# Kernel optimization log

Measured on AMD Instinct MI355X. Metric: run time of the kernel, lower is better.

The kernel has to match this reference:

```python
import jax, jax.numpy as jnp
import numpy as np

DIM, HEADS, DH, M, PINV_ITERS, RES_K = 512, 8, 64, 256, 6, 33

def layernorm(x, w, b, eps=1e-5):
    mu = jnp.mean(x, -1, keepdims=True)
    var = jnp.var(x, -1, keepdims=True)
    return (x - mu) * jax.lax.rsqrt(var + eps) * w + b

def pinv_iter(x, iters=PINV_ITERS):
    # Moore-Penrose iterative pseudo-inverse (lucidrains nystrom-attention)
    ax = jnp.abs(x)
    z = jnp.swapaxes(x, -1, -2) / (jnp.max(ax.sum(-1)) * jnp.max(ax.sum(-2)))
    I = jnp.eye(x.shape[-1], dtype=x.dtype)
    for _ in range(iters):
        xz = x @ z
        z = 0.25 * z @ (13 * I - xz @ (15 * I - xz @ (7 * I - xz)))
    return z

def _core(x, w_qkv):
    b, n, _ = x.shape
    pad = (M - n % M) % M            # Nystrom pads at the FRONT to a multiple of m=256
    xp = jnp.pad(x, ((0, 0), (pad, 0), (0, 0)))
    npad = n + pad
    q, k, v = jnp.split(xp @ w_qkv, 3, axis=-1)
    split_heads = lambda t: t.reshape(b, npad, HEADS, DH).transpose(0, 2, 1, 3)
    q = split_heads(q) * (DH ** -0.5)
    k, v = split_heads(k), split_heads(v)
    l = npad // M                    # tokens per landmark
    q_l = q.reshape(b, HEADS, M, l, DH).mean(3)
    k_l = k.reshape(b, HEADS, M, l, DH).mean(3)
    return q, k, v, q_l, k_l, pad, n

def nystrom_out(x, w_qkv, w_out, b_out, res_kernel):
    q, k, v, q_l, k_l, pad, n = _core(x, w_qkv)
    attn1 = jax.nn.softmax(jnp.einsum('bhid,bhjd->bhij', q, k_l), -1)    # (b,h,N,M)
    attn2 = jax.nn.softmax(jnp.einsum('bhid,bhjd->bhij', q_l, k_l), -1)  # (b,h,M,M)
    attn3 = jax.nn.softmax(jnp.einsum('bhid,bhjd->bhij', q_l, k), -1)    # (b,h,M,N)
    out = (attn1 @ pinv_iter(attn2)) @ (attn3 @ v)
    # depthwise residual conv over sequence dim, per head
    out = out + jax.lax.conv_general_dilated(
        v, res_kernel, (1, 1), [(RES_K // 2, RES_K // 2), (0, 0)],
        dimension_numbers=('NCHW', 'OIHW', 'NCHW'), feature_group_count=HEADS)
    b = out.shape[0]
    out = out.transpose(0, 2, 1, 3).reshape(b, -1, HEADS * DH) @ w_out + b_out
    return out[:, -n:]

def nystrom_cls_row(x, w_qkv):
    # cls-token (query index pad, head 0) row of attn1 @ pinv(attn2) @ attn3;
    # identical math to the full (n x n) matrix row the torch code slices out.
    q, k, v, q_l, k_l, pad, n = _core(x, w_qkv)
    q0, k0, ql0, kl0 = q[:, 0], k[:, 0], q_l[:, 0], k_l[:, 0]
    attn2 = jax.nn.softmax(ql0 @ jnp.swapaxes(kl0, -1, -2), -1)   # (b,M,M)
    attn3 = jax.nn.softmax(ql0 @ jnp.swapaxes(k0, -1, -2), -1)    # (b,M,N)
    row1 = jax.nn.softmax(jnp.einsum('bd,bjd->bj', q0[:, pad], kl0), -1)
    row = jnp.einsum('bj,bjk->bk', row1, pinv_iter(attn2))
    row = jnp.einsum('bk,bkn->bn', row, attn3)                    # (b, N_padded)
    return row, pad

def dwconv(x, k, b, p):
    y = jax.lax.conv_general_dilated(x, k, (1, 1), [(p, p), (p, p)],
        dimension_numbers=('NCHW', 'OIHW', 'NCHW'), feature_group_count=x.shape[1])
    return y + b[None, :, None, None]

def leff(x, k7, b7, k5, b5, k3, b3, Hs, Ws):
    cls_t, feat = x[:, :1], x[:, 1:]
    B, N, C = feat.shape
    img = feat.transpose(0, 2, 1).reshape(B, C, Hs, Ws)
    y = dwconv(img, k7, b7, 3) + img + dwconv(img, k5, b5, 2) + dwconv(img, k3, b3, 1)
    y = y.reshape(B, C, Hs * Ws).transpose(0, 2, 1)
    return jnp.concatenate([cls_t, y], axis=1)

def setup_inputs():
    key = jax.random.key(0)
    ks = iter(jax.random.split(key, 32))
    n, n_classes = 22500, 2
    p = {}
    p['h'] = jax.random.normal(next(ks), (n, 1024), jnp.float32)
    p['fc1_w'] = jax.random.normal(next(ks), (1024, DIM), jnp.float32) * 0.02
    p['fc1_b'] = jnp.zeros((DIM,), jnp.float32)
    p['cls_token'] = jax.random.normal(next(ks), (1, 1, DIM), jnp.float32)
    for pre in ('l1', 'l2'):
        p[pre + '_ln_w'] = jnp.ones((DIM,), jnp.float32)
        p[pre + '_ln_b'] = jnp.zeros((DIM,), jnp.float32)
        p[pre + '_wqkv'] = jax.random.normal(next(ks), (DIM, 3 * HEADS * DH), jnp.float32) * 0.02
        p[pre + '_wout'] = jax.random.normal(next(ks), (HEADS * DH, DIM), jnp.float32) * 0.02
        p[pre + '_bout'] = jnp.zeros((DIM,), jnp.float32)
        p[pre + '_resk'] = jax.random.normal(next(ks), (HEADS, 1, RES_K, 1), jnp.float32) * 0.05
    for kk in (7, 5, 3):
        p['leff_k%d' % kk] = jax.random.normal(next(ks), (DIM, 1, kk, kk), jnp.float32) * 0.05
        p['leff_b%d' % kk] = jnp.zeros((DIM,), jnp.float32)
    p['norm_w'] = jnp.ones((DIM,), jnp.float32)
    p['norm_b'] = jnp.zeros((DIM,), jnp.float32)
    p['fc2_w'] = jax.random.normal(next(ks), (DIM, n_classes), jnp.float32) * 0.02
    p['fc2_b'] = jnp.zeros((n_classes,), jnp.float32)
    return p

def reference(h, fc1_w, fc1_b, cls_token,
              l1_ln_w, l1_ln_b, l1_wqkv, l1_wout, l1_bout, l1_resk,
              leff_k7, leff_b7, leff_k5, leff_b5, leff_k3, leff_b3,
              l2_ln_w, l2_ln_b, l2_wqkv, l2_wout, l2_bout, l2_resk,
              norm_w, norm_b, fc2_w, fc2_b):
    x = h[None]                                   # (1, n, 1024)
    n = x.shape[1]
    x = jax.nn.relu(x @ fc1_w + fc1_b)            # (1, n, 512)
    Hs = int(np.ceil(np.sqrt(n)))                 # 150 for n=22500
    add_len = Hs * Hs - n
    if add_len > 0:
        x = jnp.concatenate([x, x[:, :add_len]], axis=1)
    x = jnp.concatenate([jnp.broadcast_to(cls_token, (1, 1, DIM)), x], axis=1)
    # TransLayer 1
    x = x + nystrom_out(layernorm(x, l1_ln_w, l1_ln_b), l1_wqkv, l1_wout, l1_bout, l1_resk)
    # LeFF positional layer
    x = leff(x, leff_k7, leff_b7, leff_k5, leff_b5, leff_k3, leff_b3, Hs, Hs)
    # TransLayer 2 (first call in TransMIL.forward)
    h2 = x + nystrom_out(layernorm(x, l2_ln_w, l2_ln_b), l2_wqkv, l2_wout, l2_bout, l2_resk)
    # TransLayer 2 second call: residual update then attention matrix of updated state
    h3 = h2 + nystrom_out(layernorm(h2, l2_ln_w, l2_ln_b), l2_wqkv, l2_wout, l2_bout, l2_resk)
    row, pad = nystrom_cls_row(layernorm(h3, l2_ln_w, l2_ln_b), l2_wqkv)
    A = row[0, pad + 1: pad + 1 + n][:, None]     # (n, 1) cls->instance attention
    hf = layernorm(h2, norm_w, norm_b)[:, 0]      # (1, 512)
    logits = hf @ fc2_w + fc2_b                   # (1, n_classes)
    Y_prob = jax.nn.softmax(logits, -1)
    return logits, Y_prob, A
```

## Files before the change

### kernel.cpp

```cpp
#include <hip/hip_runtime.h>

#define NTOK 22500
#define N1   22501
#define NPAD 22528
#define PADR 27
#define DIM  512
#define NH   8
#define DHD  64
#define MM   256
#define LLM  88
#define HSZ  150
#define CSZ  256
#define NCH  88

typedef short bf16x8 __attribute__((ext_vector_type(8)));
typedef float f32x4  __attribute__((ext_vector_type(4)));

union U8 { bf16x8 v; unsigned short u[8]; };

__device__ __forceinline__ unsigned short f2b(float f){
  unsigned int u = __float_as_uint(f);
  unsigned int r = u + 0x7fffu + ((u>>16)&1u);
  return (unsigned short)(r>>16);
}
__device__ __forceinline__ float bf2f(unsigned short u){
  return __uint_as_float(((unsigned int)u)<<16);
}
__device__ __forceinline__ bf16x8 cvt8(float4 a, float4 b){
  U8 u;
  u.u[0]=f2b(a.x); u.u[1]=f2b(a.y); u.u[2]=f2b(a.z); u.u[3]=f2b(a.w);
  u.u[4]=f2b(b.x); u.u[5]=f2b(b.y); u.u[6]=f2b(b.z); u.u[7]=f2b(b.w);
  return u.v;
}

__device__ __forceinline__ float waveSum(float v){
#pragma unroll
  for (int o=32;o>0;o>>=1) v += __shfl_down(v,o);
  return v;
}
__device__ __forceinline__ float waveMax(float v){
#pragma unroll
  for (int o=32;o>0;o>>=1) v = fmaxf(v,__shfl_down(v,o));
  return v;
}
__device__ __forceinline__ float blockSum256(float v, float* sb){
  v = waveSum(v);
  __syncthreads();
  if ((threadIdx.x&63)==0) sb[threadIdx.x>>6]=v;
  __syncthreads();
  return sb[0]+sb[1]+sb[2]+sb[3];
}
__device__ __forceinline__ float blockMax256(float v, float* sb){
  v = waveMax(v);
  __syncthreads();
  if ((threadIdx.x&63)==0) sb[threadIdx.x>>6]=v;
  __syncthreads();
  return fmaxf(fmaxf(sb[0],sb[1]),fmaxf(sb[2],sb[3]));
}

__global__ void k_wT(const float* __restrict__ W, unsigned short* __restrict__ Bt, int K, int N)
{
  __shared__ float tile[32][33];
  int tx = threadIdx.x&31, ty = threadIdx.x>>5;
  int k0 = blockIdx.x*32, n0 = blockIdx.y*32;
#pragma unroll
  for (int i=0;i<4;++i){
    int k = k0+ty+i*8;
    if (k<K && n0+tx<N) tile[ty+i*8][tx] = W[(size_t)k*N + n0+tx];
  }
  __syncthreads();
#pragma unroll
  for (int i=0;i<4;++i){
    int n = n0+ty+i*8, k = k0+tx;
    if (n<N && k<K) Bt[(size_t)n*K + k] = f2b(tile[tx][ty+i*8]);
  }
}

template<int MODE>
__global__ __launch_bounds__(256) void k_gemm(const float* __restrict__ A,
    const unsigned short* __restrict__ Bt, const float* __restrict__ bias,
    float* __restrict__ Cf, float* __restrict__ C2,
    unsigned short* __restrict__ Q_, unsigned short* __restrict__ K_,
    unsigned short* __restrict__ V_, unsigned short* __restrict__ Vt_, int Kd)
{
  __shared__ unsigned short As[128*64];
  __shared__ unsigned short Bs[128*64];
  const int tid = threadIdx.x;
  const int m0 = blockIdx.x*128, n0 = blockIdx.y*128;
  const int lane = tid & 63;
  const int wid = tid >> 6;
  const int wm = (wid>>1)*64, wn = (wid&1)*64;
  f32x4 acc[4][4] = {};
  for (int k0=0; k0<Kd; k0+=64){
    __syncthreads();
#pragma unroll
    for (int i=0;i<8;++i){
      int g = i*256 + tid;
      int row = g>>4, k4 = (g&15)*4;
      float4 v = make_float4(0.f,0.f,0.f,0.f);
      int gm = m0 + row;
      if (MODE==0){ if (gm < NTOK) v = *(const float4*)(A + (size_t)gm*Kd + k0 + k4); }
      else if (MODE==1 || MODE==3){ if (gm >= PADR) v = *(const float4*)(A + (size_t)(gm-PADR)*Kd + k0 + k4); }
      else { if (gm < N1) v = *(const float4*)(A + (size_t)(gm+PADR)*Kd + k0 + k4); }
      ushort4 h4;
      h4.x=f2b(v.x); h4.y=f2b(v.y); h4.z=f2b(v.z); h4.w=f2b(v.w);
      *(ushort4*)(&As[row*64 + (k4 ^ ((row&7)<<3))]) = h4;
    }
#pragma unroll
    for (int i=0;i<8;++i){
      int g = i*256 + tid;
      int col = g>>4, k4 = (g&15)*4;
      int vn = n0 + col;
      if (MODE==3) vn = (vn<64) ? vn : vn+448;
      ushort4 h4 = *(const ushort4*)(Bt + (size_t)vn*Kd + k0 + k4);
      *(ushort4*)(&Bs[col*64 + (k4 ^ ((col&7)<<3))]) = h4;
    }
    __syncthreads();
#pragma unroll
    for (int ks=0; ks<2; ++ks){
      const int kk = ks*32 + (lane>>4)*8;
      bf16x8 af[4], bfm[4];
#pragma unroll
      for (int t=0;t<4;++t){
        int r = wm + t*16 + (lane&15);
        af[t] = *(bf16x8*)(&As[r*64 + (kk ^ ((r&7)<<3))]);
        int c = wn + t*16 + (lane&15);
        bfm[t] = *(bf16x8*)(&Bs[c*64 + (kk ^ ((c&7)<<3))]);
      }
#pragma unroll
      for (int mt=0;mt<4;++mt)
#pragma unroll
        for (int nt=0;nt<4;++nt)
          acc[mt][nt] = __builtin_amdgcn_mfma_f32_16x16x32_bf16(af[mt], bfm[nt], acc[mt][nt], 0,0,0);
    }
  }
  const int rbase = (lane>>4)*4;
  const int cl = lane&15;
#pragma unroll
  for (int mt=0;mt<4;++mt){
#pragma unroll
    for (int r=0;r<4;++r){
      int gm = m0 + wm + mt*16 + rbase + r;
#pragma unroll
      for (int nt=0;nt<4;++nt){
        int gn = n0 + wn + nt*16 + cl;
        float v = acc[mt][nt][r];
        if (MODE==0){
          if (gm < NTOK){ float o = v + bias[gn]; Cf[(size_t)(1+gm)*DIM + gn] = o>0.f?o:0.f; }
        } else if (MODE==1){
          int sec = gn>>9, hh=(gn>>6)&7, d=gn&63;
          if (sec==0) Q_[((size_t)hh*NPAD+gm)*DHD + d] = f2b(v*0.125f);
          else if (sec==1) K_[((size_t)hh*NPAD+gm)*DHD + d] = f2b(v);
          else {
            unsigned short bv = f2b(v);
            V_[((size_t)hh*NPAD+gm)*DHD + d] = bv;
            Vt_[((size_t)hh*DHD + d)*NPAD + gm] = bv;
          }
        } else if (MODE==2){
          if (gm < N1) Cf[(size_t)gm*DIM + gn] += v + bias[gn];
        } else {
          if (gn < 64) Cf[(size_t)gm*DHD + gn] = v*0.125f;
          else         C2[(size_t)gm*DHD + (gn-64)] = v;
        }
      }
    }
  }
}

__global__ void k_setcls(float* __restrict__ X, const float* __restrict__ cls){
  int i = blockIdx.x*256 + threadIdx.x;
  if (i < DIM) X[i] = cls[i];
}
__global__ void k_copy(float* __restrict__ d, const float* __restrict__ s, size_t n){
  size_t i = (size_t)blockIdx.x*256 + threadIdx.x;
  if (i<n) d[i]=s[i];
}

__global__ void k_ln(const float* __restrict__ X, float* __restrict__ Y,
                     const float* __restrict__ w, const float* __restrict__ b)
{
  __shared__ float sb[4];
  const float* x = X + (size_t)blockIdx.x*DIM;
  float* y = Y + (size_t)blockIdx.x*DIM;
  int t = threadIdx.x;
  float a0=x[t], a1=x[t+256];
  float s = blockSum256(a0+a1, sb);
  float q = blockSum256(a0*a0+a1*a1, sb);
  float mean = s*(1.f/512.f);
  float var = q*(1.f/512.f) - mean*mean;
  float rstd = rsqrtf(var+1e-5f);
  y[t]     = (a0-mean)*rstd*w[t]+b[t];
  y[t+256] = (a1-mean)*rstd*w[t+256]+b[t+256];
}

__global__ void k_landmark_b(const unsigned short* __restrict__ src, float* __restrict__ dst)
{
  int hm = blockIdx.x; int h = hm>>8, m = hm&255; int d = threadIdx.x;
  const unsigned short* base = src + ((size_t)h*NPAD + (size_t)m*LLM)*DHD + d;
  float s = 0.f;
  for (int j=0;j<LLM;++j) s += bf2f(base[(size_t)j*DHD]);
  dst[((size_t)h*MM + m)*DHD + d] = s * (1.f/(float)LLM);
}
__global__ void k_landmark(const float* __restrict__ src, float* __restrict__ dst)
{
  int hm = blockIdx.x; int h = hm>>8, m = hm&255; int d = threadIdx.x;
  const float* base = src + ((size_t)h*NPAD + (size_t)m*LLM)*DHD + d;
  float s = 0.f;
  for (int j=0;j<LLM;++j) s += base[(size_t)j*DHD];
  dst[((size_t)h*MM + m)*DHD + d] = s * (1.f/(float)LLM);
}

__global__ __launch_bounds__(64) void k_nt64(const float* __restrict__ A,
    const float* __restrict__ B, float* __restrict__ C,
    long sA, long sB, long sC, int Nr)
{
  int lane = threadIdx.x;
  int n0 = blockIdx.x*64, m0 = blockIdx.y*64;
  A += (size_t)blockIdx.z*sA; B += (size_t)blockIdx.z*sB; C += (size_t)blockIdx.z*sC;
  f32x4 acc[4][4] = {};
#pragma unroll
  for (int ks=0;ks<2;++ks){
    int kk = ks*32 + (lane>>4)*8;
    bf16x8 af[4], bfr[4];
#pragma unroll
    for (int mt=0;mt<4;++mt){
      const float* p = A + (size_t)(m0+mt*16+(lane&15))*64 + kk;
      af[mt] = cvt8(*(const float4*)p, *(const float4*)(p+4));
    }
#pragma unroll
    for (int nt=0;nt<4;++nt){
      const float* p = B + (size_t)(n0+nt*16+(lane&15))*64 + kk;
      bfr[nt] = cvt8(*(const float4*)p, *(const float4*)(p+4));
    }
#pragma unroll
    for (int mt=0;mt<4;++mt)
#pragma unroll
      for (int nt=0;nt<4;++nt)
        acc[mt][nt] = __builtin_amdgcn_mfma_f32_16x16x32_bf16(af[mt], bfr[nt], acc[mt][nt], 0,0,0);
  }
#pragma unroll
  for (int mt=0;mt<4;++mt)
#pragma unroll
    for (int r=0;r<4;++r){
      int row = m0+mt*16+(lane>>4)*4+r;
#pragma unroll
      for (int nt=0;nt<4;++nt){
        int col = n0+nt*16+(lane&15);
        C[(size_t)row*Nr + col] = acc[mt][nt][r];
      }
    }
}

template<int PM>
__global__ __launch_bounds__(256) void k_pgemm(const float* __restrict__ A,
    const float* __restrict__ Bt, float* __restrict__ C, float* __restrict__ Ct,
    unsigned short* __restrict__ Ctb, float dc, float alpha)
{
  __shared__ unsigned short As[64*256];
  __shared__ unsigned short Bs[64*256];
  const int tid = threadIdx.x, lane = tid&63, wid = tid>>6;
  const int n0 = blockIdx.x*64, m0 = blockIdx.y*64;
  const float* Ab = A + (size_t)blockIdx.z*65536;
  const float* Bb = Bt + (size_t)blockIdx.z*(PM==2?16384:65536);
  for (int i=tid; i<4096; i+=256){
    int r = i>>6, c4 = (i&63)*4;
    float4 va = *(const float4*)(Ab + (size_t)(m0+r)*256 + c4);
    ushort4 ua; ua.x=f2b(va.x); ua.y=f2b(va.y); ua.z=f2b(va.z); ua.w=f2b(va.w);
    *(ushort4*)(&As[r*256 + (c4 ^ ((r&7)<<3))]) = ua;
    float4 vb = *(const float4*)(Bb + (size_t)(n0+r)*256 + c4);
    ushort4 ub; ub.x=f2b(vb.x); ub.y=f2b(vb.y); ub.z=f2b(vb.z); ub.w=f2b(vb.w);
    *(ushort4*)(&Bs[r*256 + (c4 ^ ((r&7)<<3))]) = ub;
  }
  __syncthreads();
  const int wm = (wid>>1)*32, wn = (wid&1)*32;
  f32x4 acc[2][2] = {};
#pragma unroll
  for (int ks=0;ks<8;++ks){
    int kk = ks*32 + (lane>>4)*8;
    bf16x8 af[2], bfr[2];
#pragma unroll
    for (int t=0;t<2;++t){
      int rr = wm + t*16 + (lane&15);
      af[t] = *(const bf16x8*)(&As[rr*256 + (kk ^ ((rr&7)<<3))]);
      int cc = wn + t*16 + (lane&15);
      bfr[t] = *(const bf16x8*)(&Bs[cc*256 + (kk ^ ((cc&7)<<3))]);
    }
#pragma unroll
    for (int mt=0;mt<2;++mt)
#pragma unroll
      for (int nt=0;nt<2;++nt)
        acc[mt][nt] = __builtin_amdgcn_mfma_f32_16x16x32_bf16(af[mt], bfr[nt], acc[mt][nt], 0,0,0);
  }
#pragma unroll
  for (int mt=0;mt<2;++mt)
#pragma unroll
    for (int r=0;r<4;++r){
      int row = m0 + wm + mt*16 + (lane>>4)*4 + r;
#pragma unroll
      for (int nt=0;nt<2;++nt){
        int col = n0 + wn + nt*16 + (lane&15);
        float v = acc[mt][nt][r];
        if (PM==1) v = alpha*(dc*Ab[(size_t)row*256+col] - v);
        if (PM==2){
          Ctb[(size_t)blockIdx.z*16384 + (size_t)col*256 + row] = f2b(v);
        } else {
          C [(size_t)blockIdx.z*65536 + (size_t)row*256 + col] = v;
          Ct[(size_t)blockIdx.z*65536 + (size_t)col*256 + row] = v;
        }
      }
    }
}

__global__ void k_softmax256(float* __restrict__ S)
{
  __shared__ float sb[4];
  float* row = S + ((size_t)blockIdx.x<<8);
  float x = row[threadIdx.x];
  float m = blockMax256(x, sb);
  float e = __expf(x-m);
  float s = blockSum256(e, sb);
  row[threadIdx.x] = e/s;
}
__global__ void k_rcsum(const float* __restrict__ A2, float* __restrict__ sums, int nb)
{
  __shared__ float sb[4];
  int b = blockIdx.x >> 8, r = blockIdx.x & 255;
  const float* Ab = A2 + ((size_t)b<<16);
  float v = (blockIdx.y==0) ? Ab[((size_t)r<<8) + threadIdx.x]
                            : Ab[((size_t)threadIdx.x<<8) + r];
  float s = blockSum256(v, sb);
  if (threadIdx.x==0) sums[(size_t)blockIdx.y*nb + blockIdx.x] = s;
}
__global__ void k_scale(const float* __restrict__ sums, float* __restrict__ scl, int nb)
{
  __shared__ float sb[4];
  float mr=-1e30f, mc=-1e30f;
  for (int i=threadIdx.x;i<nb;i+=256) mr = fmaxf(mr, sums[i]);
  for (int i=threadIdx.x;i<nb;i+=256) mc = fmaxf(mc, sums[nb+i]);
  mr = blockMax256(mr, sb);
  mc = blockMax256(mc, sb);
  if (threadIdx.x==0) scl[0] = 1.f/(mr*mc);
}
__global__ void k_z0(const float* __restrict__ A2, float* __restrict__ Z, float* __restrict__ Zt,
                     const float* __restrict__ scl)
{
  size_t idx = (size_t)blockIdx.x*256 + threadIdx.x;
  size_t b = idx>>16; int i=(int)((idx>>8)&255), j=(int)(idx&255);
  float s = scl[0];
  float v = A2[idx]*s;
  Zt[idx] = v;
  Z[(b<<16)+((size_t)j<<8)+i] = v;
}

__global__ __launch_bounds__(256) void k_attn3(const float* __restrict__ QL,
    const unsigned short* __restrict__ Kb, const unsigned short* __restrict__ Vt,
    float* __restrict__ Pmax, float* __restrict__ Psum, unsigned short* __restrict__ Pacc)
{
  __shared__ unsigned short Ks[64*64];
  __shared__ unsigned short Vs[64*64];
  __shared__ unsigned short Ps[4*64*64];
  int h = blockIdx.y, cx = blockIdx.x;
  int tid = threadIdx.x, wid = tid>>6, lane = tid&63;
  bf16x8 aq[4][2];
#pragma unroll
  for (int mt=0;mt<4;++mt){
    const float* qp = QL + ((size_t)h*MM + wid*64 + mt*16 + (lane&15))*DHD;
#pragma unroll
    for (int ks=0;ks<2;++ks){
      int kk = ks*32 + (lane>>4)*8;
      aq[mt][ks] = cvt8(*(const float4*)(qp+kk), *(const float4*)(qp+kk+4));
    }
  }
  float m_[4][4], l_[4][4];
  f32x4 acc[4][4] = {};
#pragma unroll
  for (int mt=0;mt<4;++mt)
#pragma unroll
    for (int r=0;r<4;++r){ m_[mt][r] = -1e30f; l_[mt][r] = 0.f; }

  unsigned short* Pw = &Ps[wid*4096];
  for (int t=0;t<4;++t){
    int kb0 = cx*CSZ + t*64;
    __syncthreads();
    for (int i=tid;i<1024;i+=256){
      int rr = i>>4, c4 = (i&15)*4;
      ushort4 ku = *(const ushort4*)(Kb + ((size_t)h*NPAD + kb0 + rr)*DHD + c4);
      *(ushort4*)(&Ks[rr*64 + (c4 ^ ((rr&7)<<3))]) = ku;
      ushort4 vu = *(const ushort4*)(Vt + ((size_t)h*DHD + rr)*NPAD + kb0 + c4);
      *(ushort4*)(&Vs[rr*64 + (c4 ^ ((rr&7)<<3))]) = vu;
    }
    __syncthreads();
    f32x4 s[4][4] = {};
#pragma unroll
    for (int ks=0;ks<2;++ks){
      int kk = ks*32 + (lane>>4)*8;
      bf16x8 kbf[4];
#pragma unroll
      for (int nt=0;nt<4;++nt){
        int key = nt*16 + (lane&15);
        kbf[nt] = *(const bf16x8*)(&Ks[key*64 + (kk ^ ((key&7)<<3))]);
      }
#pragma unroll
      for (int mt=0;mt<4;++mt)
#pragma unroll
        for (int nt=0;nt<4;++nt)
          s[mt][nt] = __builtin_amdgcn_mfma_f32_16x16x32_bf16(aq[mt][ks], kbf[nt], s[mt][nt], 0,0,0);
    }
#pragma unroll
    for (int mt=0;mt<4;++mt){
#pragma unroll
      for (int r=0;r<4;++r){
        float mx = fmaxf(fmaxf(s[mt][0][r], s[mt][1][r]), fmaxf(s[mt][2][r], s[mt][3][r]));
#pragma unroll
        for (int off=8;off>=1;off>>=1) mx = fmaxf(mx, __shfl_xor(mx, off));
        float mn = fmaxf(m_[mt][r], mx);
        float f = __expf(m_[mt][r]-mn);
        float la = 0.f;
#pragma unroll
        for (int nt=0;nt<4;++nt){ float p=__expf(s[mt][nt][r]-mn); s[mt][nt][r]=p; la+=p; }
#pragma unroll
        for (int off=8;off>=1;off>>=1) la += __shfl_xor(la, off);
        l_[mt][r] = l_[mt][r]*f + la;
        m_[mt][r] = mn;
#pragma unroll
        for (int dt=0;dt<4;++dt) acc[mt][dt][r] *= f;
      }
    }
#pragma unroll
    for (int mt=0;mt<4;++mt)
#pragma unroll
      for (int r=0;r<4;++r){
        int row = mt*16 + (lane>>4)*4 + r;
        int sw = (row&7)<<3;
#pragma unroll
        for (int nt=0;nt<4;++nt){
          int col = nt*16 + (lane&15);
          Pw[row*64 + (col ^ sw)] = f2b(s[mt][nt][r]);
        }
      }
#pragma unroll
    for (int ks=0;ks<2;++ks){
      int kk = ks*32 + (lane>>4)*8;
      bf16x8 pa[4], vb[4];
#pragma unroll
      for (int mt=0;mt<4;++mt){
        int arow = mt*16 + (lane&15);
        pa[mt] = *(const bf16x8*)(&Pw[arow*64 + (kk ^ ((arow&7)<<3))]);
      }
#pragma unroll
      for (int dt=0;dt<4;++dt){
        int d = dt*16 + (lane&15);
        vb[dt] = *(const bf16x8*)(&Vs[d*64 + (kk ^ ((d&7)<<3))]);
      }
#pragma unroll
      for (int mt=0;mt<4;++mt)
#pragma unroll
        for (int dt=0;dt<4;++dt)
          acc[mt][dt] = __builtin_amdgcn_mfma_f32_16x16x32_bf16(pa[mt], vb[dt], acc[mt][dt], 0,0,0);
    }
  }
  size_t pbase = ((size_t)h*NCH + cx)*MM;
#pragma unroll
  for (int mt=0;mt<4;++mt)
#pragma unroll
    for (int r=0;r<4;++r){
      int row = wid*64 + mt*16 + (lane>>4)*4 + r;
      if ((lane&15)==0){ Pmax[pbase+row]=m_[mt][r]; Psum[pbase+row]=l_[mt][r]; }
#pragma unroll
      for (int dt=0;dt<4;++dt)
        Pacc[(pbase+row)*DHD + dt*16+(lane&15)] = f2b(acc[mt][dt][r]);
    }
}

__global__ void k_attn3_merge(const float* __restrict__ Pmax, const float* __restrict__ Psum,
    const unsigned short* __restrict__ Pacc, float* __restrict__ A3Vt)
{
  int hm = blockIdx.x; int h = hm>>8, m = hm&255; int d = threadIdx.x;
  float gm = -1e30f;
  for (int c=0;c<NCH;++c) gm = fmaxf(gm, Pmax[((size_t)h*NCH+c)*MM+m]);
  float tot=0.f, acc=0.f;
  for (int c=0;c<NCH;++c){
    size_t pi = ((size_t)h*NCH+c)*MM+m;
    float w = __expf(Pmax[pi]-gm);
    tot += Psum[pi]*w;
    acc += bf2f(Pacc[pi*DHD+d])*w;
  }
  A3Vt[((size_t)h*DHD + d)*MM + m] = acc/tot;
}

__global__ __launch_bounds__(256) void k_attn1(const unsigned short* __restrict__ Qb,
    const float* __restrict__ KL, const unsigned short* __restrict__ WmT,
    float* __restrict__ OH)
{
  __shared__ unsigned short KWs[64*256];
  __shared__ unsigned short Ps[64*256];
  int h = blockIdx.y, tid = threadIdx.x;
  int wid = tid>>6, lane = tid&63;
  int q0 = blockIdx.x*64;
  for (int i=tid; i<4096; i+=256){
    int lm = i>>4, k4 = (i&15)*4;
    float4 v = *(const float4*)(KL + ((size_t)h*MM + lm)*DHD + k4);
    ushort4 u; u.x=f2b(v.x); u.y=f2b(v.y); u.z=f2b(v.z); u.w=f2b(v.w);
    *(ushort4*)(&KWs[lm*64 + (k4 ^ ((lm&7)<<3))]) = u;
  }
  bf16x8 aq[2];
  const unsigned short* qp = Qb + ((size_t)h*NPAD + q0 + wid*16 + (lane&15))*DHD;
#pragma unroll
  for (int ks=0;ks<2;++ks)
    aq[ks] = *(const bf16x8*)(qp + ks*32 + (lane>>4)*8);
  __syncthreads();
  f32x4 s[16];
#pragma unroll
  for (int nt=0;nt<16;++nt) s[nt] = (f32x4){0.f,0.f,0.f,0.f};
#pragma unroll
  for (int ks=0;ks<2;++ks){
    int kk = ks*32 + (lane>>4)*8;
#pragma unroll
    for (int nt=0;nt<16;++nt){
      int col = nt*16 + (lane&15);
      bf16x8 b = *(const bf16x8*)(&KWs[col*64 + (kk ^ ((col&7)<<3))]);
      s[nt] = __builtin_amdgcn_mfma_f32_16x16x32_bf16(aq[ks], b, s[nt], 0,0,0);
    }
  }
  float rcp[4];
#pragma unroll
  for (int r=0;r<4;++r){
    float m = -1e30f;
#pragma unroll
    for (int nt=0;nt<16;++nt) m = fmaxf(m, s[nt][r]);
#pragma unroll
    for (int off=8;off>=1;off>>=1) m = fmaxf(m, __shfl_xor(m, off));
    float l = 0.f;
#pragma unroll
    for (int nt=0;nt<16;++nt){ float p=__expf(s[nt][r]-m); s[nt][r]=p; l+=p; }
#pragma unroll
    for (int off=8;off>=1;off>>=1) l += __shfl_xor(l, off);
    rcp[r] = 1.f/l;
  }
  int prow_base = wid*16 + (lane>>4)*4;
#pragma unroll
  for (int nt=0;nt<16;++nt){
    int col = nt*16 + (lane&15);
#pragma unroll
    for (int r=0;r<4;++r){
      int row = prow_base + r;
      Ps[row*256 + (col ^ ((row&7)<<3))] = f2b(s[nt][r]);
    }
  }
  __syncthreads();
  for (int i=tid; i<4096; i+=256){
    int d = i>>6, k4 = (i&63)*4;
    ushort4 u = *(const ushort4*)(WmT + ((size_t)h*DHD + d)*MM + k4);
    *(ushort4*)(&KWs[d*256 + (k4 ^ ((d&7)<<3))]) = u;
  }
  __syncthreads();
  f32x4 acc[4] = {};
  int arow = wid*16 + (lane&15);
#pragma unroll
  for (int ks=0;ks<8;++ks){
    int kk = ks*32 + (lane>>4)*8;
    bf16x8 a = *(const bf16x8*)(&Ps[arow*256 + (kk ^ ((arow&7)<<3))]);
#pragma unroll
    for (int dt=0;dt<4;++dt){
      int d = dt*16 + (lane&15);
      bf16x8 b = *(const bf16x8*)(&KWs[d*256 + (kk ^ ((d&7)<<3))]);
      acc[dt] = __builtin_amdgcn_mfma_f32_16x16x32_bf16(a, b, acc[dt], 0,0,0);
    }
  }
#pragma unroll
  for (int r=0;r<4;++r){
    int row = q0 + prow_base + r;
    float* op = OH + (size_t)row*DIM + h*DHD;
#pragma unroll
    for (int dt=0;dt<4;++dt)
      op[dt*16 + (lane&15)] = acc[dt][r]*rcp[r];
  }
}

#define SCBLK 32
__global__ __launch_bounds__(256) void k_seqconv(const unsigned short* __restrict__ Vb,
    const float* __restrict__ resk, float* __restrict__ OH)
{
  __shared__ unsigned short Vs[64*512];
  int tid = threadIdx.x;
  int p0 = blockIdx.x*SCBLK;
  for (int i=tid; i<16384; i+=256){
    int pl = i>>8, c2 = i&255;
    int gp = p0 - 16 + pl;
    int hh = c2>>5, d2 = (c2&31)*2;
    ushort2 v = make_ushort2(0,0);
    if (gp>=0 && gp<NPAD) v = *(const ushort2*)(Vb + ((size_t)hh*NPAD+gp)*DHD + d2);
    *(ushort2*)(&Vs[pl*512 + c2*2]) = v;
  }
  __syncthreads();
  int h = tid>>5;
  float kr[33];
#pragma unroll
  for (int r=0;r<33;++r) kr[r] = resk[h*33+r];
  for (int pl=0; pl<SCBLK; ++pl){
    float s0=0.f, s1=0.f;
#pragma unroll
    for (int r=0;r<33;++r){
      ushort2 v = *(const ushort2*)(&Vs[(pl+r)*512 + tid*2]);
      s0 += bf2f(v.x)*kr[r];
      s1 += bf2f(v.y)*kr[r];
    }
    size_t o = (size_t)(p0+pl)*DIM + tid*2;
    float2 cur = *(float2*)(OH + o);
    cur.x += s0; cur.y += s1;
    *(float2*)(OH + o) = cur;
  }
}

__global__ void k_tfwd(const float* __restrict__ X, float* __restrict__ T)
{
  __shared__ float tile[32][33];
  int tx = threadIdx.x & 31, ty = threadIdx.x >> 5;
  int s0 = blockIdx.x*32, c0 = blockIdx.y*32;
  for (int yy=0; yy<4; ++yy){
    int s = s0 + ty + yy*8;
    if (s < NTOK) tile[ty+yy*8][tx] = X[(size_t)(1+s)*DIM + c0+tx];
  }
  __syncthreads();
  for (int yy=0; yy<4; ++yy){
    int c = c0 + ty + yy*8;
    int s = s0 + tx;
    if (s < NTOK) T[(size_t)c*NTOK + s] = tile[tx][ty+yy*8];
  }
}
__global__ void k_tbwd(const float* __restrict__ T, float* __restrict__ X)
{
  __shared__ float tile[32][33];
  int tx = threadIdx.x & 31, ty = threadIdx.x >> 5;
  int s0 = blockIdx.x*32, c0 = blockIdx.y*32;
  for (int yy=0; yy<4; ++yy){
    int c = c0 + ty + yy*8, s = s0 + tx;
    if (s < NTOK) tile[ty+yy*8][tx] = T[(size_t)c*NTOK + s];
  }
  __syncthreads();
  for (int yy=0; yy<4; ++yy){
    int s = s0 + ty + yy*8, c = c0 + tx;
    if (s < NTOK) X[(size_t)(1+s)*DIM + c] = tile[tx][ty+yy*8];
  }
}
__global__ __launch_bounds__(256) void k_leff(const float* __restrict__ T,
    const float* __restrict__ k7, const float* __restrict__ b7,
    const float* __restrict__ k5, const float* __restrict__ b5,
    const float* __restrict__ k3, const float* __restrict__ b3,
    float* __restrict__ T2)
{
  __shared__ float tile[21*21];
  int c = blockIdx.y;
  int ti = blockIdx.x/10, tj = blockIdx.x%10;
  int i0 = ti*15-3, j0 = tj*15-3;
  const float* img = T + (size_t)c*NTOK;
  for (int idx=threadIdx.x; idx<441; idx+=256){
    int ii = idx/21, jj = idx%21;
    int gi = i0+ii, gj = j0+jj;
    tile[idx] = (gi>=0 && gi<HSZ && gj>=0 && gj<HSZ) ? img[gi*HSZ+gj] : 0.f;
  }
  __syncthreads();
  if (threadIdx.x < 225){
    int li = threadIdx.x/15, lj = threadIdx.x%15;
    int gi = ti*15+li, gj = tj*15+lj;
    float acc = tile[(li+3)*21 + (lj+3)] + b7[c]+b5[c]+b3[c];
    const float* w7 = k7 + c*49;
#pragma unroll
    for (int a=0;a<7;++a)
#pragma unroll
      for (int bb=0;bb<7;++bb) acc += tile[(li+a)*21 + (lj+bb)]*w7[a*7+bb];
    const float* w5 = k5 + c*25;
#pragma unroll
    for (int a=0;a<5;++a)
#pragma unroll
      for (int bb=0;bb<5;++bb) acc += tile[(li+1+a)*21 + (lj+1+bb)]*w5[a*5+bb];
    const float* w3 = k3 + c*9;
#pragma unroll
    for (int a=0;a<3;++a)
#pragma unroll
      for (int bb=0;bb<3;++bb) acc += tile[(li+2+a)*21 + (lj+2+bb)]*w3[a*3+bb];
    T2[(size_t)c*NTOK + gi*HSZ+gj] = acc;
  }
}

__global__ void k_row1(const float* __restrict__ Q0, const float* __restrict__ KL0,
                       float* __restrict__ row1)
{
  __shared__ float sb[4];
  __shared__ float qv[64];
  int t = threadIdx.x;
  if (t<64) qv[t] = Q0[PADR*DHD + t];
  __syncthreads();
  float l = 0.f;
#pragma unroll
  for (int d=0;d<64;++d) l += qv[d]*KL0[(size_t)t*DHD+d];
  float m = blockMax256(l, sb);
  float e = __expf(l-m);
  float s = blockSum256(e, sb);
  row1[t] = e/s;
}
__global__ void k_rz(const float* __restrict__ row1, const float* __restrict__ Zt,
                     float* __restrict__ rz)
{
  __shared__ float r1[256];
  int t = threadIdx.x;
  r1[t] = row1[t];
  __syncthreads();
  float s = 0.f;
  for (int k2=0;k2<256;++k2) s += r1[k2]*Zt[(size_t)t*MM + k2];
  rz[t] = s;
}
__global__ void k_rowstat(const float* __restrict__ L0, float* __restrict__ mx, float* __restrict__ se)
{
  __shared__ float sb[4];
  const float* row = L0 + (size_t)blockIdx.x*NPAD;
  float m = -1e30f;
  for (int i=threadIdx.x;i<NPAD;i+=256) m = fmaxf(m, row[i]);
  m = blockMax256(m, sb);
  float s = 0.f;
  for (int i=threadIdx.x;i<NPAD;i+=256) s += __expf(row[i]-m);
  s = blockSum256(s, sb);
  if (threadIdx.x==0){ mx[blockIdx.x]=m; se[blockIdx.x]=s; }
}
__global__ void k_aout(const float* __restrict__ L0, const float* __restrict__ rz,
    const float* __restrict__ mx, const float* __restrict__ se, float* __restrict__ out)
{
  __shared__ float wk[256], mk[256];
  int t = threadIdx.x;
  wk[t] = rz[t]/se[t];
  mk[t] = mx[t];
  __syncthreads();
  int p = blockIdx.x*256 + t;
  if (p >= NTOK) return;
  size_t pp = (size_t)(PADR+1+p);
  float a = 0.f;
  for (int k2=0;k2<256;++k2) a += wk[k2]*__expf(L0[(size_t)k2*NPAD+pp]-mk[k2]);
  out[4+p] = a;
}
__global__ void k_final(const float* __restrict__ H2r, const float* __restrict__ nw,
    const float* __restrict__ nbb, const float* __restrict__ w2, const float* __restrict__ b2,
    float* __restrict__ out)
{
  __shared__ float sb[4];
  __shared__ float hf[512];
  int t = threadIdx.x;
  float x0 = H2r[t], x1 = H2r[256+t];
  float s = blockSum256(x0+x1, sb);
  float q = blockSum256(x0*x0+x1*x1, sb);
  float mean = s*(1.f/512.f);
  float var = q*(1.f/512.f) - mean*mean;
  float rstd = rsqrtf(var+1e-5f);
  hf[t]     = (x0-mean)*rstd*nw[t]+nbb[t];
  hf[256+t] = (x1-mean)*rstd*nw[256+t]+nbb[256+t];
  __syncthreads();
  float p0 = hf[t]*w2[t*2]   + hf[256+t]*w2[(256+t)*2];
  float p1 = hf[t]*w2[t*2+1] + hf[256+t]*w2[(256+t)*2+1];
  p0 = blockSum256(p0, sb);
  p1 = blockSum256(p1, sb);
  if (t==0){
    float l0 = p0+b2[0], l1 = p1+b2[1];
    float m = fmaxf(l0,l1);
    float e0 = __expf(l0-m), e1 = __expf(l1-m), si = 1.f/(e0+e1);
    out[0]=l0; out[1]=l1; out[2]=e0*si; out[3]=e1*si;
  }
}

struct Bufs {
  float *X,*Y,*QL,*KL,*A2,*Z0,*Z0t,*Z1,*Z1t,*XZ,*XZt,*T1,*T1t,*T2,*T2t;
  float *A3Vt,*sums,*scl,*Pmax,*Psum;
  unsigned short *Qb,*Kb,*Vb,*Vt,*WmT,*Pacc;
};

static void run_pinv(const float* A2, Bufs& b, int NB, hipStream_t st,
                     float** outZ, float** outZt)
{
  dim3 g(4,4,NB);
  float *Zc=b.Z0, *Zct=b.Z0t, *Zn=b.Z1, *Znt=b.Z1t;
  for (int it=0; it<6; ++it){
    k_pgemm<0><<<g,256,0,st>>>(A2, Zct, b.XZ, b.XZt, nullptr, 0.f, 1.f);
    k_pgemm<1><<<g,256,0,st>>>(b.XZ, b.XZt, b.T1, b.T1t, nullptr, 7.f, 1.f);
    k_pgemm<1><<<g,256,0,st>>>(b.XZ, b.T1t, b.T2, b.T2t, nullptr, 15.f, 1.f);
    k_pgemm<1><<<g,256,0,st>>>(Zc, b.T2t, Zn, Znt, nullptr, 13.f, 0.25f);
    float* t1=Zc; Zc=Zn; Zn=t1;
    float* t2=Zct; Zct=Znt; Znt=t2;
  }
  *outZ = Zc; *outZt = Zct;
}

static void nystrom_layer(Bufs& b, const float* lnw, const float* lnb,
    const unsigned short* wqkvT, const unsigned short* woutT,
    const float* bout, const float* resk, hipStream_t st)
{
  k_ln<<<N1,256,0,st>>>(b.X, b.Y, lnw, lnb);
  k_gemm<1><<<dim3(NPAD/128,12),256,0,st>>>(b.Y, wqkvT, nullptr, nullptr, nullptr,
      b.Qb, b.Kb, b.Vb, b.Vt, DIM);
  k_landmark_b<<<NH*MM,64,0,st>>>(b.Qb, b.QL);
  k_landmark_b<<<NH*MM,64,0,st>>>(b.Kb, b.KL);
  k_nt64<<<dim3(4,4,NH),64,0,st>>>(b.QL, b.KL, b.A2,
      (long)MM*DHD,(long)MM*DHD,(long)MM*MM, MM);
  k_softmax256<<<NH*MM,256,0,st>>>(b.A2);
  k_rcsum<<<dim3(NH*MM,2),256,0,st>>>(b.A2, b.sums, NH*MM);
  k_scale<<<1,256,0,st>>>(b.sums, b.scl, NH*MM);
  k_z0<<<NH*MM*MM/256,256,0,st>>>(b.A2, b.Z0, b.Z0t, b.scl);
  float *Zc, *Zct;
  run_pinv(b.A2, b, NH, st, &Zc, &Zct);
  k_attn3<<<dim3(NCH,NH),256,0,st>>>(b.QL, b.Kb, b.Vt, b.Pmax, b.Psum, b.Pacc);
  k_attn3_merge<<<NH*MM,64,0,st>>>(b.Pmax, b.Psum, b.Pacc, b.A3Vt);
  k_pgemm<2><<<dim3(1,4,NH),256,0,st>>>(Zc, b.A3Vt, nullptr, nullptr, b.WmT, 0.f, 1.f);
  k_attn1<<<dim3(NPAD/64,NH),256,0,st>>>(b.Qb, b.KL, b.WmT, b.Y);
  k_seqconv<<<NPAD/SCBLK,256,0,st>>>(b.Vb, resk, b.Y);
  k_gemm<2><<<dim3(176,4),256,0,st>>>(b.Y, woutT, bout, b.X, nullptr,
      nullptr, nullptr, nullptr, nullptr, DIM);
}

extern "C" void kernel_launch(void* const* d_in, const int* in_sizes, int n_in,
                              void* d_out, int out_size, void* d_ws, size_t ws_size,
                              hipStream_t stream)
{
  (void)n_in; (void)out_size;
  bool sig_order = (in_sizes[10] == 25088);
  int iL2 = sig_order ? 16 : 10;
  int iLf = sig_order ? 10 : 16;

  const float* h       = (const float*)d_in[0];
  const float* fc1_w   = (const float*)d_in[1];
  const float* fc1_b   = (const float*)d_in[2];
  const float* cls_tok = (const float*)d_in[3];
  const float* l1_lnw  = (const float*)d_in[4];
  const float* l1_lnb  = (const float*)d_in[5];
  const float* l1_wqkv = (const float*)d_in[6];
  const float* l1_wout = (const float*)d_in[7];
  const float* l1_bout = (const float*)d_in[8];
  const float* l1_resk = (const float*)d_in[9];
  const float* l2_lnw  = (const float*)d_in[iL2+0];
  const float* l2_lnb  = (const float*)d_in[iL2+1];
  const float* l2_wqkv = (const float*)d_in[iL2+2];
  const float* l2_wout = (const float*)d_in[iL2+3];
  const float* l2_bout = (const float*)d_in[iL2+4];
  const float* l2_resk = (const float*)d_in[iL2+5];
  const float* k7 = (const float*)d_in[iLf+0];
  const float* b7 = (const float*)d_in[iLf+1];
  const float* k5 = (const float*)d_in[iLf+2];
  const float* b5 = (const float*)d_in[iLf+3];
  const float* k3 = (const float*)d_in[iLf+4];
  const float* b3 = (const float*)d_in[iLf+5];
  const float* nw = (const float*)d_in[22];
  const float* nbb= (const float*)d_in[23];
  const float* w2 = (const float*)d_in[24];
  const float* b2 = (const float*)d_in[25];
  float* out = (float*)d_out;

  char* base = (char*)d_ws;
  auto allocF = [&](size_t n)->float*{
    float* p=(float*)base; base += ((n*sizeof(float)+255)&~(size_t)255); return p; };
  auto allocU = [&](size_t n)->unsigned short*{
    unsigned short* p=(unsigned short*)base; base += ((n*sizeof(unsigned short)+255)&~(size_t)255); return p; };

  const size_t S = (size_t)NPAD*DIM;
  const size_t SQ = (size_t)MM*MM;
  Bufs b;
  b.X  = allocF(S);
  b.Y  = allocF(S);
  b.Qb = allocU(S);
  b.Kb = allocU(S);
  b.Vb = allocU(S);
  b.Vt = allocU(S);
  b.QL = allocF((size_t)NH*MM*DHD);
  b.KL = allocF((size_t)NH*MM*DHD);
  b.A2 = allocF((size_t)NH*SQ);
  b.Z0 = allocF((size_t)NH*SQ);  b.Z0t = allocF((size_t)NH*SQ);
  b.Z1 = allocF((size_t)NH*SQ);  b.Z1t = allocF((size_t)NH*SQ);
  b.XZ = allocF((size_t)NH*SQ);  b.XZt = allocF((size_t)NH*SQ);
  b.T1 = allocF((size_t)NH*SQ);  b.T1t = allocF((size_t)NH*SQ);
  b.T2 = allocF((size_t)NH*SQ);  b.T2t = allocF((size_t)NH*SQ);
  b.A3Vt = allocF((size_t)NH*MM*DHD);
  b.WmT  = allocU((size_t)NH*MM*DHD);
  b.sums = allocF(2*(size_t)NH*MM);
  b.scl  = allocF(16);
  b.Pmax = allocF((size_t)NH*NCH*MM);
  b.Psum = allocF((size_t)NH*NCH*MM);
  b.Pacc = allocU((size_t)NH*NCH*MM*DHD);
  unsigned short* fc1T   = allocU((size_t)DIM*1024);
  unsigned short* wqkvT1 = allocU((size_t)1536*DIM);
  unsigned short* wqkvT2 = allocU((size_t)1536*DIM);
  unsigned short* woutT1 = allocU((size_t)DIM*DIM);
  unsigned short* woutT2 = allocU((size_t)DIM*DIM);
  float* Q0   = allocF((size_t)NPAD*DHD);
  float* K0   = allocF((size_t)NPAD*DHD);
  float* row1 = allocF(256);
  float* rzv  = allocF(256);
  float* mxv  = allocF(256);
  float* sev  = allocF(256);
  float* h2row= allocF(512);
  if ((size_t)(base - (char*)d_ws) > ws_size) return;

  k_wT<<<dim3(32,16),256,0,stream>>>(fc1_w, fc1T, 1024, DIM);
  k_wT<<<dim3(16,48),256,0,stream>>>(l1_wqkv, wqkvT1, DIM, 1536);
  k_wT<<<dim3(16,48),256,0,stream>>>(l2_wqkv, wqkvT2, DIM, 1536);
  k_wT<<<dim3(16,16),256,0,stream>>>(l1_wout, woutT1, DIM, DIM);
  k_wT<<<dim3(16,16),256,0,stream>>>(l2_wout, woutT2, DIM, DIM);

  k_gemm<0><<<dim3(176,4),256,0,stream>>>(h, fc1T, fc1_b, b.X, nullptr,
      nullptr, nullptr, nullptr, nullptr, 1024);
  k_setcls<<<2,256,0,stream>>>(b.X, cls_tok);

  nystrom_layer(b, l1_lnw, l1_lnb, wqkvT1, woutT1, l1_bout, l1_resk, stream);
  k_tfwd<<<dim3(704,16),256,0,stream>>>(b.X, b.Y);
  k_leff<<<dim3(100,512),256,0,stream>>>(b.Y, k7,b7,k5,b5,k3,b3, (float*)b.Z0);
  k_tbwd<<<dim3(704,16),256,0,stream>>>((float*)b.Z0, b.X);

  nystrom_layer(b, l2_lnw, l2_lnb, wqkvT2, woutT2, l2_bout, l2_resk, stream);
  k_copy<<<2,256,0,stream>>>(h2row, b.X, 512);

  nystrom_layer(b, l2_lnw, l2_lnb, wqkvT2, woutT2, l2_bout, l2_resk, stream);

  k_ln<<<N1,256,0,stream>>>(b.X, b.Y, l2_lnw, l2_lnb);
  k_gemm<3><<<dim3(176,1),256,0,stream>>>(b.Y, wqkvT2, nullptr, Q0, K0,
      nullptr, nullptr, nullptr, nullptr, DIM);
  k_landmark<<<MM,64,0,stream>>>(Q0, b.QL);
  k_landmark<<<MM,64,0,stream>>>(K0, b.KL);
  k_nt64<<<dim3(4,4,1),64,0,stream>>>(b.QL, b.KL, b.A2, 0,0,0, MM);
  k_softmax256<<<MM,256,0,stream>>>(b.A2);
  k_rcsum<<<dim3(MM,2),256,0,stream>>>(b.A2, b.sums, MM);
  k_scale<<<1,256,0,stream>>>(b.sums, b.scl, MM);
  k_z0<<<MM*MM/256,256,0,stream>>>(b.A2, b.Z0, b.Z0t, b.scl);
  float *Zc, *Zct;
  run_pinv(b.A2, b, 1, stream, &Zc, &Zct);
  k_row1<<<1,256,0,stream>>>(Q0, b.KL, row1);
  k_rz<<<1,256,0,stream>>>(row1, Zct, rzv);
  k_nt64<<<dim3(NPAD/64,4,1),64,0,stream>>>(b.QL, K0, b.Y, 0,0,0, NPAD);
  k_rowstat<<<MM,256,0,stream>>>(b.Y, mxv, sev);
  k_aout<<<88,256,0,stream>>>(b.Y, rzv, mxv, sev, out);
  k_final<<<1,256,0,stream>>>(h2row, nw, nbb, w2, b2, out);
}
```

Measured before the change: 2.740 ms.

## Store intermediates as bf16 and stage QKV epilogue through LDS for coalesced writes

Most intermediate buffers (LayerNorm output, attention output, landmarks, pinv iterates, the attn3·V result, the LeFF transposes) now hold bf16 instead of fp32, and the GEMMs load them directly without converting. The QKV GEMM epilogue is staged through shared memory so it writes 16-byte vectors, and the strided V-transpose store is moved into a separate tiled transpose kernel. Some pinv iterations no longer write the non-transposed copy. This halves memory traffic on the large activations, at the cost of extra rounding in the pseudo-inverse iteration and the residual paths.

```diff
diff --git a/kernel.cpp b/kernel.cpp
--- a/kernel.cpp
+++ b/kernel.cpp
@@ -15,6 +15,7 @@
 
 typedef short bf16x8 __attribute__((ext_vector_type(8)));
 typedef float f32x4  __attribute__((ext_vector_type(4)));
+typedef unsigned short us;
 
 union U8 { bf16x8 v; unsigned short u[8]; };
 
@@ -58,7 +59,7 @@
   return fmaxf(fmaxf(sb[0],sb[1]),fmaxf(sb[2],sb[3]));
 }
 
-__global__ void k_wT(const float* __restrict__ W, unsigned short* __restrict__ Bt, int K, int N)
+__global__ void k_wT(const float* __restrict__ W, us* __restrict__ Bt, int K, int N)
 {
   __shared__ float tile[32][33];
   int tx = threadIdx.x&31, ty = threadIdx.x>>5;
@@ -76,15 +77,34 @@
   }
 }
 
+__global__ void k_vT(const us* __restrict__ V, us* __restrict__ Vt)
+{
+  __shared__ us tile[32][33];
+  int tx = threadIdx.x&31, ty = threadIdx.x>>5;
+  int p0 = blockIdx.x*32;
+  int h = blockIdx.y>>1, d0 = (blockIdx.y&1)*32;
+#pragma unroll
+  for (int i=0;i<4;++i){
+    int p = p0+ty+i*8;
+    tile[ty+i*8][tx] = V[((size_t)h*NPAD+p)*DHD + d0+tx];
+  }
+  __syncthreads();
+#pragma unroll
+  for (int i=0;i<4;++i){
+    int d = d0+ty+i*8;
+    Vt[((size_t)h*DHD+d)*NPAD + p0+tx] = tile[tx][ty+i*8];
+  }
+}
+
 template<int MODE>
-__global__ __launch_bounds__(256) void k_gemm(const float* __restrict__ A,
-    const unsigned short* __restrict__ Bt, const float* __restrict__ bias,
+__global__ __launch_bounds__(256) void k_gemm(const float* __restrict__ Af,
+    const us* __restrict__ Ab, const us* __restrict__ Bt, const float* __restrict__ bias,
     float* __restrict__ Cf, float* __restrict__ C2,
-    unsigned short* __restrict__ Q_, unsigned short* __restrict__ K_,
-    unsigned short* __restrict__ V_, unsigned short* __restrict__ Vt_, int Kd)
-{
-  __shared__ unsigned short As[128*64];
-  __shared__ unsigned short Bs[128*64];
+    us* __restrict__ Q_, us* __restrict__ K_, us* __restrict__ V_, int Kd)
+{
+  __shared__ us SM[16384];
+  us* As = SM;
+  us* Bs = SM + 8192;
   const int tid = threadIdx.x;
   const int m0 = blockIdx.x*128, n0 = blockIdx.y*128;
   const int lane = tid & 63;
@@ -97,13 +117,18 @@
     for (int i=0;i<8;++i){
       int g = i*256 + tid;
       int row = g>>4, k4 = (g&15)*4;
-      float4 v = make_float4(0.f,0.f,0.f,0.f);
       int gm = m0 + row;
-      if (MODE==0){ if (gm < NTOK) v = *(const float4*)(A + (size_t)gm*Kd + k0 + k4); }
-      else if (MODE==1 || MODE==3){ if (gm >= PADR) v = *(const float4*)(A + (size_t)(gm-PADR)*Kd + k0 + k4); }
-      else { if (gm < N1) v = *(const float4*)(A + (size_t)(gm+PADR)*Kd + k0 + k4); }
-      ushort4 h4;
-      h4.x=f2b(v.x); h4.y=f2b(v.y); h4.z=f2b(v.z); h4.w=f2b(v.w);
+      ushort4 h4 = make_ushort4(0,0,0,0);
+      if (MODE==0){
+        if (gm < NTOK){
+          float4 v = *(const float4*)(Af + (size_t)gm*Kd + k0 + k4);
+          h4.x=f2b(v.x); h4.y=f2b(v.y); h4.z=f2b(v.z); h4.w=f2b(v.w);
+        }
+      } else if (MODE==1 || MODE==3){
+        if (gm >= PADR) h4 = *(const ushort4*)(Ab + (size_t)(gm-PADR)*Kd + k0 + k4);
+      } else {
+        if (gm < N1) h4 = *(const ushort4*)(Ab + (size_t)(gm+PADR)*Kd + k0 + k4);
+      }
       *(ushort4*)(&As[row*64 + (k4 ^ ((row&7)<<3))]) = h4;
     }
 #pragma unroll
@@ -136,31 +161,49 @@
   }
   const int rbase = (lane>>4)*4;
   const int cl = lane&15;
-#pragma unroll
-  for (int mt=0;mt<4;++mt){
-#pragma unroll
-    for (int r=0;r<4;++r){
-      int gm = m0 + wm + mt*16 + rbase + r;
-#pragma unroll
-      for (int nt=0;nt<4;++nt){
-        int gn = n0 + wn + nt*16 + cl;
-        float v = acc[mt][nt][r];
-        if (MODE==0){
-          if (gm < NTOK){ float o = v + bias[gn]; Cf[(size_t)(1+gm)*DIM + gn] = o>0.f?o:0.f; }
-        } else if (MODE==1){
-          int sec = gn>>9, hh=(gn>>6)&7, d=gn&63;
-          if (sec==0) Q_[((size_t)hh*NPAD+gm)*DHD + d] = f2b(v*0.125f);
-          else if (sec==1) K_[((size_t)hh*NPAD+gm)*DHD + d] = f2b(v);
-          else {
-            unsigned short bv = f2b(v);
-            V_[((size_t)hh*NPAD+gm)*DHD + d] = bv;
-            Vt_[((size_t)hh*DHD + d)*NPAD + gm] = bv;
+  if (MODE==1){
+    const int sec = blockIdx.y>>2;
+    const float sc = sec==0 ? 0.125f : 1.f;
+    __syncthreads();
+#pragma unroll
+    for (int mt=0;mt<4;++mt)
+#pragma unroll
+      for (int r=0;r<4;++r){
+        int row = wm + mt*16 + rbase + r;
+#pragma unroll
+        for (int nt=0;nt<4;++nt){
+          int col = wn + nt*16 + cl;
+          SM[row*128 + col] = f2b(acc[mt][nt][r]*sc);
+        }
+      }
+    __syncthreads();
+    us* dst = sec==0 ? Q_ : (sec==1 ? K_ : V_);
+#pragma unroll
+    for (int i=0;i<8;++i){
+      int v8 = i*256 + tid;
+      int row = v8>>4, c8 = (v8&15)*8;
+      int gm = m0 + row, gn = n0 + c8;
+      int hh = (gn>>6)&7, d = gn&63;
+      *(bf16x8*)(dst + ((size_t)hh*NPAD+gm)*DHD + d) = *(bf16x8*)(&SM[row*128 + c8]);
+    }
+  } else {
+#pragma unroll
+    for (int mt=0;mt<4;++mt){
+#pragma unroll
+      for (int r=0;r<4;++r){
+        int gm = m0 + wm + mt*16 + rbase + r;
+#pragma unroll
+        for (int nt=0;nt<4;++nt){
+          int gn = n0 + wn + nt*16 + cl;
+          float v = acc[mt][nt][r];
+          if (MODE==0){
+            if (gm < NTOK){ float o = v + bias[gn]; Cf[(size_t)(1+gm)*DIM + gn] = o>0.f?o:0.f; }
+          } else if (MODE==2){
+            if (gm < N1) Cf[(size_t)gm*DIM + gn] += v + bias[gn];
+          } else {
+            if (gn < 64) Cf[(size_t)gm*DHD + gn] = v*0.125f;
+            else         C2[(size_t)gm*DHD + (gn-64)] = v;
           }
-        } else if (MODE==2){
-          if (gm < N1) Cf[(size_t)gm*DIM + gn] += v + bias[gn];
-        } else {
-          if (gn < 64) Cf[(size_t)gm*DHD + gn] = v*0.125f;
-          else         C2[(size_t)gm*DHD + (gn-64)] = v;
         }
       }
     }
@@ -176,12 +219,12 @@
   if (i<n) d[i]=s[i];
 }
 
-__global__ void k_ln(const float* __restrict__ X, float* __restrict__ Y,
+__global__ void k_ln(const float* __restrict__ X, us* __restrict__ Y,
                      const float* __restrict__ w, const float* __restrict__ b)
 {
   __shared__ float sb[4];
   const float* x = X + (size_t)blockIdx.x*DIM;
-  float* y = Y + (size_t)blockIdx.x*DIM;
+  us* y = Y + (size_t)blockIdx.x*DIM;
   int t = threadIdx.x;
   float a0=x[t], a1=x[t+256];
   float s = blockSum256(a0+a1, sb);
@@ -189,17 +232,17 @@
   float mean = s*(1.f/512.f);
   float var = q*(1.f/512.f) - mean*mean;
   float rstd = rsqrtf(var+1e-5f);
-  y[t]     = (a0-mean)*rstd*w[t]+b[t];
-  y[t+256] = (a1-mean)*rstd*w[t+256]+b[t+256];
-}
-
-__global__ void k_landmark_b(const unsigned short* __restrict__ src, float* __restrict__ dst)
+  y[t]     = f2b((a0-mean)*rstd*w[t]+b[t]);
+  y[t+256] = f2b((a1-mean)*rstd*w[t+256]+b[t+256]);
+}
+
+__global__ void k_landmark_b(const us* __restrict__ src, us* __restrict__ dst)
 {
   int hm = blockIdx.x; int h = hm>>8, m = hm&255; int d = threadIdx.x;
-  const unsigned short* base = src + ((size_t)h*NPAD + (size_t)m*LLM)*DHD + d;
+  const us* base = src + ((size_t)h*NPAD + (size_t)m*LLM)*DHD + d;
   float s = 0.f;
   for (int j=0;j<LLM;++j) s += bf2f(base[(size_t)j*DHD]);
-  dst[((size_t)h*MM + m)*DHD + d] = s * (1.f/(float)LLM);
+  dst[((size_t)h*MM + m)*DHD + d] = f2b(s * (1.f/(float)LLM));
 }
 __global__ void k_landmark(const float* __restrict__ src, float* __restrict__ dst)
 {
@@ -251,25 +294,58 @@
     }
 }
 
+__global__ __launch_bounds__(64) void k_nt64b(const us* __restrict__ A,
+    const us* __restrict__ B, float* __restrict__ C,
+    long sA, long sB, long sC, int Nr)
+{
+  int lane = threadIdx.x;
+  int n0 = blockIdx.x*64, m0 = blockIdx.y*64;
+  A += (size_t)blockIdx.z*sA; B += (size_t)blockIdx.z*sB; C += (size_t)blockIdx.z*sC;
+  f32x4 acc[4][4] = {};
+#pragma unroll
+  for (int ks=0;ks<2;++ks){
+    int kk = ks*32 + (lane>>4)*8;
+    bf16x8 af[4], bfr[4];
+#pragma unroll
+    for (int mt=0;mt<4;++mt)
+      af[mt] = *(const bf16x8*)(A + (size_t)(m0+mt*16+(lane&15))*64 + kk);
+#pragma unroll
+    for (int nt=0;nt<4;++nt)
+      bfr[nt] = *(const bf16x8*)(B + (size_t)(n0+nt*16+(lane&15))*64 + kk);
+#pragma unroll
+    for (int mt=0;mt<4;++mt)
+#pragma unroll
+      for (int nt=0;nt<4;++nt)
+        acc[mt][nt] = __builtin_amdgcn_mfma_f32_16x16x32_bf16(af[mt], bfr[nt], acc[mt][nt], 0,0,0);
+  }
+#pragma unroll
+  for (int mt=0;mt<4;++mt)
+#pragma unroll
+    for (int r=0;r<4;++r){
+      int row = m0+mt*16+(lane>>4)*4+r;
+#pragma unroll
+      for (int nt=0;nt<4;++nt){
+        int col = n0+nt*16+(lane&15);
+        C[(size_t)row*Nr + col] = acc[mt][nt][r];
+      }
+    }
+}
+
 template<int PM>
-__global__ __launch_bounds__(256) void k_pgemm(const float* __restrict__ A,
-    const float* __restrict__ Bt, float* __restrict__ C, float* __restrict__ Ct,
-    unsigned short* __restrict__ Ctb, float dc, float alpha)
-{
-  __shared__ unsigned short As[64*256];
-  __shared__ unsigned short Bs[64*256];
+__global__ __launch_bounds__(256) void k_pgemm(const us* __restrict__ A,
+    const us* __restrict__ Bt, us* __restrict__ C, us* __restrict__ Ct,
+    float dc, float alpha, int writeC)
+{
+  __shared__ us As[64*256];
+  __shared__ us Bs[64*256];
   const int tid = threadIdx.x, lane = tid&63, wid = tid>>6;
   const int n0 = blockIdx.x*64, m0 = blockIdx.y*64;
-  const float* Ab = A + (size_t)blockIdx.z*65536;
-  const float* Bb = Bt + (size_t)blockIdx.z*(PM==2?16384:65536);
+  const us* Ab = A + (size_t)blockIdx.z*65536;
+  const us* Bb = Bt + (size_t)blockIdx.z*(PM==2?16384:65536);
   for (int i=tid; i<4096; i+=256){
     int r = i>>6, c4 = (i&63)*4;
-    float4 va = *(const float4*)(Ab + (size_t)(m0+r)*256 + c4);
-    ushort4 ua; ua.x=f2b(va.x); ua.y=f2b(va.y); ua.z=f2b(va.z); ua.w=f2b(va.w);
-    *(ushort4*)(&As[r*256 + (c4 ^ ((r&7)<<3))]) = ua;
-    float4 vb = *(const float4*)(Bb + (size_t)(n0+r)*256 + c4);
-    ushort4 ub; ub.x=f2b(vb.x); ub.y=f2b(vb.y); ub.z=f2b(vb.z); ub.w=f2b(vb.w);
-    *(ushort4*)(&Bs[r*256 + (c4 ^ ((r&7)<<3))]) = ub;
+    *(ushort4*)(&As[r*256 + (c4 ^ ((r&7)<<3))]) = *(const ushort4*)(Ab + (size_t)(m0+r)*256 + c4);
+    *(ushort4*)(&Bs[r*256 + (c4 ^ ((r&7)<<3))]) = *(const ushort4*)(Bb + (size_t)(n0+r)*256 + c4);
   }
   __syncthreads();
   const int wm = (wid>>1)*32, wn = (wid&1)*32;
@@ -300,18 +376,19 @@
       for (int nt=0;nt<2;++nt){
         int col = n0 + wn + nt*16 + (lane&15);
         float v = acc[mt][nt][r];
-        if (PM==1) v = alpha*(dc*Ab[(size_t)row*256+col] - v);
+        if (PM==1) v = alpha*(dc*bf2f(Ab[(size_t)row*256+col]) - v);
         if (PM==2){
-          Ctb[(size_t)blockIdx.z*16384 + (size_t)col*256 + row] = f2b(v);
+          Ct[(size_t)blockIdx.z*16384 + (size_t)col*256 + row] = f2b(v);
         } else {
-          C [(size_t)blockIdx.z*65536 + (size_t)row*256 + col] = v;
-          Ct[(size_t)blockIdx.z*65536 + (size_t)col*256 + row] = v;
+          us bv = f2b(v);
+          if (PM==0 || writeC) C[(size_t)blockIdx.z*65536 + (size_t)row*256 + col] = bv;
+          Ct[(size_t)blockIdx.z*65536 + (size_t)col*256 + row] = bv;
         }
       }
     }
 }
 
-__global__ void k_softmax256(float* __restrict__ S)
+__global__ void k_softmax256(float* __restrict__ S, us* __restrict__ Sb)
 {
   __shared__ float sb[4];
   float* row = S + ((size_t)blockIdx.x<<8);
@@ -319,7 +396,9 @@
   float m = blockMax256(x, sb);
   float e = __expf(x-m);
   float s = blockSum256(e, sb);
-  row[threadIdx.x] = e/s;
+  float p = e/s;
+  row[threadIdx.x] = p;
+  Sb[((size_t)blockIdx.x<<8) + threadIdx.x] = f2b(p);
 }
 __global__ void k_rcsum(const float* __restrict__ A2, float* __restrict__ sums, int nb)
 {
@@ -341,35 +420,33 @@
   mc = blockMax256(mc, sb);
   if (threadIdx.x==0) scl[0] = 1.f/(mr*mc);
 }
-__global__ void k_z0(const float* __restrict__ A2, float* __restrict__ Z, float* __restrict__ Zt,
+__global__ void k_z0(const float* __restrict__ A2, us* __restrict__ Z, us* __restrict__ Zt,
                      const float* __restrict__ scl)
 {
   size_t idx = (size_t)blockIdx.x*256 + threadIdx.x;
   size_t b = idx>>16; int i=(int)((idx>>8)&255), j=(int)(idx&255);
-  float s = scl[0];
-  float v = A2[idx]*s;
-  Zt[idx] = v;
-  Z[(b<<16)+((size_t)j<<8)+i] = v;
-}
-
-__global__ __launch_bounds__(256) void k_attn3(const float* __restrict__ QL,
-    const unsigned short* __restrict__ Kb, const unsigned short* __restrict__ Vt,
-    float* __restrict__ Pmax, float* __restrict__ Psum, unsigned short* __restrict__ Pacc)
-{
-  __shared__ unsigned short Ks[64*64];
-  __shared__ unsigned short Vs[64*64];
-  __shared__ unsigned short Ps[4*64*64];
+  float v = A2[idx]*scl[0];
+  us bv = f2b(v);
+  Zt[idx] = bv;
+  Z[(b<<16)+((size_t)j<<8)+i] = bv;
+}
+
+__global__ __launch_bounds__(256) void k_attn3(const us* __restrict__ QLb,
+    const us* __restrict__ Kb, const us* __restrict__ Vt,
+    float* __restrict__ Pmax, float* __restrict__ Psum, us* __restrict__ Pacc)
+{
+  __shared__ us Ks[64*64];
+  __shared__ us Vs[64*64];
+  __shared__ us Ps[4*64*64];
   int h = blockIdx.y, cx = blockIdx.x;
   int tid = threadIdx.x, wid = tid>>6, lane = tid&63;
   bf16x8 aq[4][2];
 #pragma unroll
   for (int mt=0;mt<4;++mt){
-    const float* qp = QL + ((size_t)h*MM + wid*64 + mt*16 + (lane&15))*DHD;
-#pragma unroll
-    for (int ks=0;ks<2;++ks){
-      int kk = ks*32 + (lane>>4)*8;
-      aq[mt][ks] = cvt8(*(const float4*)(qp+kk), *(const float4*)(qp+kk+4));
-    }
+    const us* qp = QLb + ((size_t)h*MM + wid*64 + mt*16 + (lane&15))*DHD;
+#pragma unroll
+    for (int ks=0;ks<2;++ks)
+      aq[mt][ks] = *(const bf16x8*)(qp + ks*32 + (lane>>4)*8);
   }
   float m_[4][4], l_[4][4];
   f32x4 acc[4][4] = {};
@@ -378,7 +455,7 @@
 #pragma unroll
     for (int r=0;r<4;++r){ m_[mt][r] = -1e30f; l_[mt][r] = 0.f; }
 
-  unsigned short* Pw = &Ps[wid*4096];
+  us* Pw = &Ps[wid*4096];
   for (int t=0;t<4;++t){
     int kb0 = cx*CSZ + t*64;
     __syncthreads();
@@ -473,7 +550,7 @@
 }
 
 __global__ void k_attn3_merge(const float* __restrict__ Pmax, const float* __restrict__ Psum,
-    const unsigned short* __restrict__ Pacc, float* __restrict__ A3Vt)
+    const us* __restrict__ Pacc, us* __restrict__ A3Vtb)
 {
   int hm = blockIdx.x; int h = hm>>8, m = hm&255; int d = threadIdx.x;
   float gm = -1e30f;
@@ -485,26 +562,25 @@
     tot += Psum[pi]*w;
     acc += bf2f(Pacc[pi*DHD+d])*w;
   }
-  A3Vt[((size_t)h*DHD + d)*MM + m] = acc/tot;
-}
-
-__global__ __launch_bounds__(256) void k_attn1(const unsigned short* __restrict__ Qb,
-    const float* __restrict__ KL, const unsigned short* __restrict__ WmT,
-    float* __restrict__ OH)
-{
-  __shared__ unsigned short KWs[64*256];
-  __shared__ unsigned short Ps[64*256];
+  A3Vtb[((size_t)h*DHD + d)*MM + m] = f2b(acc/tot);
+}
+
+__global__ __launch_bounds__(256) void k_attn1(const us* __restrict__ Qb,
+    const us* __restrict__ KLb, const us* __restrict__ WmT,
+    us* __restrict__ OH)
+{
+  __shared__ us KWs[64*256];
+  __shared__ us Ps[64*256];
   int h = blockIdx.y, tid = threadIdx.x;
   int wid = tid>>6, lane = tid&63;
   int q0 = blockIdx.x*64;
   for (int i=tid; i<4096; i+=256){
     int lm = i>>4, k4 = (i&15)*4;
-    float4 v = *(const float4*)(KL + ((size_t)h*MM + lm)*DHD + k4);
-    ushort4 u; u.x=f2b(v.x); u.y=f2b(v.y); u.z=f2b(v.z); u.w=f2b(v.w);
-    *(ushort4*)(&KWs[lm*64 + (k4 ^ ((lm&7)<<3))]) = u;
+    *(ushort4*)(&KWs[lm*64 + (k4 ^ ((lm&7)<<3))]) =
+        *(const ushort4*)(KLb + ((size_t)h*MM + lm)*DHD + k4);
   }
   bf16x8 aq[2];
-  const unsigned short* qp = Qb + ((size_t)h*NPAD + q0 + wid*16 + (lane&15))*DHD;
+  const us* qp = Qb + ((size_t)h*NPAD + q0 + wid*16 + (lane&15))*DHD;
 #pragma unroll
   for (int ks=0;ks<2;++ks)
     aq[ks] = *(const bf16x8*)(qp + ks*32 + (lane>>4)*8);
@@ -570,18 +646,18 @@
 #pragma unroll
   for (int r=0;r<4;++r){
     int row = q0 + prow_base + r;
-    float* op = OH + (size_t)row*DIM + h*DHD;
+    us* op = OH + (size_t)row*DIM + h*DHD;
 #pragma unroll
     for (int dt=0;dt<4;++dt)
-      op[dt*16 + (lane&15)] = acc[dt][r]*rcp[r];
+      op[dt*16 + (lane&15)] = f2b(acc[dt][r]*rcp[r]);
   }
 }
 
 #define SCBLK 32
-__global__ __launch_bounds__(256) void k_seqconv(const unsigned short* __restrict__ Vb,
-    const float* __restrict__ resk, float* __restrict__ OH)
-{
-  __shared__ unsigned short Vs[64*512];
+__global__ __launch_bounds__(256) void k_seqconv(const us* __restrict__ Vb,
+    const float* __restrict__ resk, us* __restrict__ OH)
+{
+  __shared__ us Vs[64*512];
   int tid = threadIdx.x;
   int p0 = blockIdx.x*SCBLK;
   for (int i=tid; i<16384; i+=256){
@@ -606,13 +682,12 @@
       s1 += bf2f(v.y)*kr[r];
     }
     size_t o = (size_t)(p0+pl)*DIM + tid*2;
-    float2 cur = *(float2*)(OH + o);
-    cur.x += s0; cur.y += s1;
-    *(float2*)(OH + o) = cur;
-  }
-}
-
-__global__ void k_tfwd(const float* __restrict__ X, float* __restrict__ T)
+    ushort2 cur = *(ushort2*)(OH + o);
+    *(ushort2*)(OH + o) = make_ushort2(f2b(bf2f(cur.x)+s0), f2b(bf2f(cur.y)+s1));
+  }
+}
+
+__global__ void k_tfwd(const float* __restrict__ X, us* __restrict__ T)
 {
   __shared__ float tile[32][33];
   int tx = threadIdx.x & 31, ty = threadIdx.x >> 5;
@@ -625,17 +700,17 @@
   for (int yy=0; yy<4; ++yy){
     int c = c0 + ty + yy*8;
     int s = s0 + tx;
-    if (s < NTOK) T[(size_t)c*NTOK + s] = tile[tx][ty+yy*8];
-  }
-}
-__global__ void k_tbwd(const float* __restrict__ T, float* __restrict__ X)
+    if (s < NTOK) T[(size_t)c*NTOK + s] = f2b(tile[tx][ty+yy*8]);
+  }
+}
+__global__ void k_tbwd(const us* __restrict__ T, float* __restrict__ X)
 {
   __shared__ float tile[32][33];
   int tx = threadIdx.x & 31, ty = threadIdx.x >> 5;
   int s0 = blockIdx.x*32, c0 = blockIdx.y*32;
   for (int yy=0; yy<4; ++yy){
     int c = c0 + ty + yy*8, s = s0 + tx;
-    if (s < NTOK) tile[ty+yy*8][tx] = T[(size_t)c*NTOK + s];
+    if (s < NTOK) tile[ty+yy*8][tx] = bf2f(T[(size_t)c*NTOK + s]);
   }
   __syncthreads();
   for (int yy=0; yy<4; ++yy){
@@ -643,21 +718,21 @@
     if (s < NTOK) X[(size_t)(1+s)*DIM + c] = tile[tx][ty+yy*8];
   }
 }
-__global__ __launch_bounds__(256) void k_leff(const float* __restrict__ T,
+__global__ __launch_bounds__(256) void k_leff(const us* __restrict__ T,
     const float* __restrict__ k7, const float* __restrict__ b7,
     const float* __restrict__ k5, const float* __restrict__ b5,
     const float* __restrict__ k3, const float* __restrict__ b3,
-    float* __restrict__ T2)
+    us* __restrict__ T2)
 {
   __shared__ float tile[21*21];
   int c = blockIdx.y;
   int ti = blockIdx.x/10, tj = blockIdx.x%10;
   int i0 = ti*15-3, j0 = tj*15-3;
-  const float* img = T + (size_t)c*NTOK;
+  const us* img = T + (size_t)c*NTOK;
   for (int idx=threadIdx.x; idx<441; idx+=256){
     int ii = idx/21, jj = idx%21;
     int gi = i0+ii, gj = j0+jj;
-    tile[idx] = (gi>=0 && gi<HSZ && gj>=0 && gj<HSZ) ? img[gi*HSZ+gj] : 0.f;
+    tile[idx] = (gi>=0 && gi<HSZ && gj>=0 && gj<HSZ) ? bf2f(img[gi*HSZ+gj]) : 0.f;
   }
   __syncthreads();
   if (threadIdx.x < 225){
@@ -679,7 +754,7 @@
     for (int a=0;a<3;++a)
 #pragma unroll
       for (int bb=0;bb<3;++bb) acc += tile[(li+2+a)*21 + (lj+2+bb)]*w3[a*3+bb];
-    T2[(size_t)c*NTOK + gi*HSZ+gj] = acc;
+    T2[(size_t)c*NTOK + gi*HSZ+gj] = f2b(acc);
   }
 }
 
@@ -699,7 +774,7 @@
   float s = blockSum256(e, sb);
   row1[t] = e/s;
 }
-__global__ void k_rz(const float* __restrict__ row1, const float* __restrict__ Zt,
+__global__ void k_rz(const float* __restrict__ row1, const us* __restrict__ Zt,
                      float* __restrict__ rz)
 {
   __shared__ float r1[256];
@@ -707,7 +782,7 @@
   r1[t] = row1[t];
   __syncthreads();
   float s = 0.f;
-  for (int k2=0;k2<256;++k2) s += r1[k2]*Zt[(size_t)t*MM + k2];
+  for (int k2=0;k2<256;++k2) s += r1[k2]*bf2f(Zt[(size_t)t*MM + k2]);
   rz[t] = s;
 }
 __global__ void k_rowstat(const float* __restrict__ L0, float* __restrict__ mx, float* __restrict__ se)
@@ -766,51 +841,53 @@
 }
 
 struct Bufs {
-  float *X,*Y,*QL,*KL,*A2,*Z0,*Z0t,*Z1,*Z1t,*XZ,*XZt,*T1,*T1t,*T2,*T2t;
-  float *A3Vt,*sums,*scl,*Pmax,*Psum;
-  unsigned short *Qb,*Kb,*Vb,*Vt,*WmT,*Pacc;
+  float *X,*A2,*sums,*scl,*Pmax,*Psum;
+  us *Yb,*OHb,*Qb,*Kb,*Vb,*Vtb,*QLb,*KLb,*A2b;
+  us *Z0b,*Z0tb,*Z1b,*Z1tb,*XZb,*XZtb,*T1tb,*T2tb;
+  us *A3Vtb,*WmT,*Pacc;
 };
 
-static void run_pinv(const float* A2, Bufs& b, int NB, hipStream_t st,
-                     float** outZ, float** outZt)
+static void run_pinv(const us* A2b, Bufs& b, int NB, hipStream_t st,
+                     us** outZ, us** outZt)
 {
   dim3 g(4,4,NB);
-  float *Zc=b.Z0, *Zct=b.Z0t, *Zn=b.Z1, *Znt=b.Z1t;
+  us *Zc=b.Z0b, *Zct=b.Z0tb, *Zn=b.Z1b, *Znt=b.Z1tb;
   for (int it=0; it<6; ++it){
-    k_pgemm<0><<<g,256,0,st>>>(A2, Zct, b.XZ, b.XZt, nullptr, 0.f, 1.f);
-    k_pgemm<1><<<g,256,0,st>>>(b.XZ, b.XZt, b.T1, b.T1t, nullptr, 7.f, 1.f);
-    k_pgemm<1><<<g,256,0,st>>>(b.XZ, b.T1t, b.T2, b.T2t, nullptr, 15.f, 1.f);
-    k_pgemm<1><<<g,256,0,st>>>(Zc, b.T2t, Zn, Znt, nullptr, 13.f, 0.25f);
-    float* t1=Zc; Zc=Zn; Zn=t1;
-    float* t2=Zct; Zct=Znt; Znt=t2;
+    k_pgemm<0><<<g,256,0,st>>>(A2b, Zct, b.XZb, b.XZtb, 0.f, 1.f, 1);
+    k_pgemm<1><<<g,256,0,st>>>(b.XZb, b.XZtb, nullptr, b.T1tb, 7.f, 1.f, 0);
+    k_pgemm<1><<<g,256,0,st>>>(b.XZb, b.T1tb, nullptr, b.T2tb, 15.f, 1.f, 0);
+    k_pgemm<1><<<g,256,0,st>>>(Zc, b.T2tb, Zn, Znt, 13.f, 0.25f, 1);
+    us* t1=Zc; Zc=Zn; Zn=t1;
+    us* t2=Zct; Zct=Znt; Znt=t2;
   }
   *outZ = Zc; *outZt = Zct;
 }
 
 static void nystrom_layer(Bufs& b, const float* lnw, const float* lnb,
-    const unsigned short* wqkvT, const unsigned short* woutT,
+    const us* wqkvT, const us* woutT,
     const float* bout, const float* resk, hipStream_t st)
 {
-  k_ln<<<N1,256,0,st>>>(b.X, b.Y, lnw, lnb);
-  k_gemm<1><<<dim3(NPAD/128,12),256,0,st>>>(b.Y, wqkvT, nullptr, nullptr, nullptr,
-      b.Qb, b.Kb, b.Vb, b.Vt, DIM);
-  k_landmark_b<<<NH*MM,64,0,st>>>(b.Qb, b.QL);
-  k_landmark_b<<<NH*MM,64,0,st>>>(b.Kb, b.KL);
-  k_nt64<<<dim3(4,4,NH),64,0,st>>>(b.QL, b.KL, b.A2,
+  k_ln<<<N1,256,0,st>>>(b.X, b.Yb, lnw, lnb);
+  k_gemm<1><<<dim3(NPAD/128,12),256,0,st>>>(nullptr, b.Yb, wqkvT, nullptr,
+      nullptr, nullptr, b.Qb, b.Kb, b.Vb, DIM);
+  k_vT<<<dim3(NPAD/32,16),256,0,st>>>(b.Vb, b.Vtb);
+  k_landmark_b<<<NH*MM,64,0,st>>>(b.Qb, b.QLb);
+  k_landmark_b<<<NH*MM,64,0,st>>>(b.Kb, b.KLb);
+  k_nt64b<<<dim3(4,4,NH),64,0,st>>>(b.QLb, b.KLb, b.A2,
       (long)MM*DHD,(long)MM*DHD,(long)MM*MM, MM);
-  k_softmax256<<<NH*MM,256,0,st>>>(b.A2);
+  k_softmax256<<<NH*MM,256,0,st>>>(b.A2, b.A2b);
   k_rcsum<<<dim3(NH*MM,2),256,0,st>>>(b.A2, b.sums, NH*MM);
   k_scale<<<1,256,0,st>>>(b.sums, b.scl, NH*MM);
-  k_z0<<<NH*MM*MM/256,256,0,st>>>(b.A2, b.Z0, b.Z0t, b.scl);
-  float *Zc, *Zct;
-  run_pinv(b.A2, b, NH, st, &Zc, &Zct);
-  k_attn3<<<dim3(NCH,NH),256,0,st>>>(b.QL, b.Kb, b.Vt, b.Pmax, b.Psum, b.Pacc);
-  k_attn3_merge<<<NH*MM,64,0,st>>>(b.Pmax, b.Psum, b.Pacc, b.A3Vt);
-  k_pgemm<2><<<dim3(1,4,NH),256,0,st>>>(Zc, b.A3Vt, nullptr, nullptr, b.WmT, 0.f, 1.f);
-  k_attn1<<<dim3(NPAD/64,NH),256,0,st>>>(b.Qb, b.KL, b.WmT, b.Y);
-  k_seqconv<<<NPAD/SCBLK,256,0,st>>>(b.Vb, resk, b.Y);
-  k_gemm<2><<<dim3(176,4),256,0,st>>>(b.Y, woutT, bout, b.X, nullptr,
-      nullptr, nullptr, nullptr, nullptr, DIM);
+  k_z0<<<NH*MM*MM/256,256,0,st>>>(b.A2, b.Z0b, b.Z0tb, b.scl);
+  us *Zc, *Zct;
+  run_pinv(b.A2b, b, NH, st, &Zc, &Zct);
+  k_attn3<<<dim3(NCH,NH),256,0,st>>>(b.QLb, b.Kb, b.Vtb, b.Pmax, b.Psum, b.Pacc);
+  k_attn3_merge<<<NH*MM,64,0,st>>>(b.Pmax, b.Psum, b.Pacc, b.A3Vtb);
+  k_pgemm<2><<<dim3(1,4,NH),256,0,st>>>(Zc, b.A3Vtb, nullptr, b.WmT, 0.f, 1.f, 0);
+  k_attn1<<<dim3(NPAD/64,NH),256,0,st>>>(b.Qb, b.KLb, b.WmT, b.OHb);
+  k_seqconv<<<NPAD/SCBLK,256,0,st>>>(b.Vb, resk, b.OHb);
+  k_gemm<2><<<dim3(176,4),256,0,st>>>(nullptr, b.OHb, woutT, bout,
+      b.X, nullptr, nullptr, nullptr, nullptr, DIM);
 }
 
 extern "C" void kernel_launch(void* const* d_in, const int* in_sizes, int n_in,
@@ -853,40 +930,44 @@
   char* base = (char*)d_ws;
   auto allocF = [&](size_t n)->float*{
     float* p=(float*)base; base += ((n*sizeof(float)+255)&~(size_t)255); return p; };
-  auto allocU = [&](size_t n)->unsigned short*{
-    unsigned short* p=(unsigned short*)base; base += ((n*sizeof(unsigned short)+255)&~(size_t)255); return p; };
+  auto allocU = [&](size_t n)->us*{
+    us* p=(us*)base; base += ((n*sizeof(us)+255)&~(size_t)255); return p; };
 
   const size_t S = (size_t)NPAD*DIM;
   const size_t SQ = (size_t)MM*MM;
   Bufs b;
-  b.X  = allocF(S);
-  b.Y  = allocF(S);
-  b.Qb = allocU(S);
-  b.Kb = allocU(S);
-  b.Vb = allocU(S);
-  b.Vt = allocU(S);
-  b.QL = allocF((size_t)NH*MM*DHD);
-  b.KL = allocF((size_t)NH*MM*DHD);
-  b.A2 = allocF((size_t)NH*SQ);
-  b.Z0 = allocF((size_t)NH*SQ);  b.Z0t = allocF((size_t)NH*SQ);
-  b.Z1 = allocF((size_t)NH*SQ);  b.Z1t = allocF((size_t)NH*SQ);
-  b.XZ = allocF((size_t)NH*SQ);  b.XZt = allocF((size_t)NH*SQ);
-  b.T1 = allocF((size_t)NH*SQ);  b.T1t = allocF((size_t)NH*SQ);
-  b.T2 = allocF((size_t)NH*SQ);  b.T2t = allocF((size_t)NH*SQ);
-  b.A3Vt = allocF((size_t)NH*MM*DHD);
-  b.WmT  = allocU((size_t)NH*MM*DHD);
-  b.sums = allocF(2*(size_t)NH*MM);
-  b.scl  = allocF(16);
-  b.Pmax = allocF((size_t)NH*NCH*MM);
-  b.Psum = allocF((size_t)NH*NCH*MM);
-  b.Pacc = allocU((size_t)NH*NCH*MM*DHD);
-  unsigned short* fc1T   = allocU((size_t)DIM*1024);
-  unsigned short* wqkvT1 = allocU((size_t)1536*DIM);
-  unsigned short* wqkvT2 = allocU((size_t)1536*DIM);
-  unsigned short* woutT1 = allocU((size_t)DIM*DIM);
-  unsigned short* woutT2 = allocU((size_t)DIM*DIM);
+  b.X   = allocF(S);
+  b.Yb  = allocU(S);
+  b.OHb = allocU(S);
+  b.Qb  = allocU(S);
+  b.Kb  = allocU(S);
+  b.Vb  = allocU(S);
+  b.Vtb = allocU(S);
+  b.QLb = allocU((size_t)NH*MM*DHD);
+  b.KLb = allocU((size_t)NH*MM*DHD);
+  b.A2  = allocF((size_t)NH*SQ);
+  b.A2b = allocU((size_t)NH*SQ);
+  b.Z0b = allocU((size_t)NH*SQ);  b.Z0tb = allocU((size_t)NH*SQ);
+  b.Z1b = allocU((size_t)NH*SQ);  b.Z1tb = allocU((size_t)NH*SQ);
+  b.XZb = allocU((size_t)NH*SQ);  b.XZtb = allocU((size_t)NH*SQ);
+  b.T1tb= allocU((size_t)NH*SQ);
+  b.T2tb= allocU((size_t)NH*SQ);
+  b.A3Vtb = allocU((size_t)NH*MM*DHD);
+  b.WmT   = allocU((size_t)NH*MM*DHD);
+  b.sums  = allocF(2*(size_t)NH*MM);
+  b.scl   = allocF(16);
+  b.Pmax  = allocF((size_t)NH*NCH*MM);
+  b.Psum  = allocF((size_t)NH*NCH*MM);
+  b.Pacc  = allocU((size_t)NH*NCH*MM*DHD);
+  us* fc1T   = allocU((size_t)DIM*1024);
+  us* wqkvT1 = allocU((size_t)1536*DIM);
+  us* wqkvT2 = allocU((size_t)1536*DIM);
+  us* woutT1 = allocU((size_t)DIM*DIM);
+  us* woutT2 = allocU((size_t)DIM*DIM);
   float* Q0   = allocF((size_t)NPAD*DHD);
   float* K0   = allocF((size_t)NPAD*DHD);
+  float* QL0f = allocF((size_t)MM*DHD);
+  float* KL0f = allocF((size_t)MM*DHD);
   float* row1 = allocF(256);
   float* rzv  = allocF(256);
   float* mxv  = allocF(256);
@@ -900,36 +981,37 @@
   k_wT<<<dim3(16,16),256,0,stream>>>(l1_wout, woutT1, DIM, DIM);
   k_wT<<<dim3(16,16),256,0,stream>>>(l2_wout, woutT2, DIM, DIM);
 
-  k_gemm<0><<<dim3(176,4),256,0,stream>>>(h, fc1T, fc1_b, b.X, nullptr,
-      nullptr, nullptr, nullptr, nullptr, 1024);
+  k_gemm<0><<<dim3(176,4),256,0,stream>>>(h, nullptr, fc1T, fc1_b,
+      b.X, nullptr, nullptr, nullptr, nullptr, 1024);
   k_setcls<<<2,256,0,stream>>>(b.X, cls_tok);
 
   nystrom_layer(b, l1_lnw, l1_lnb, wqkvT1, woutT1, l1_bout, l1_resk, stream);
-  k_tfwd<<<dim3(704,16),256,0,stream>>>(b.X, b.Y);
-  k_leff<<<dim3(100,512),256,0,stream>>>(b.Y, k7,b7,k5,b5,k3,b3, (float*)b.Z0);
-  k_tbwd<<<dim3(704,16),256,0,stream>>>((float*)b.Z0, b.X);
+  k_tfwd<<<dim3(704,16),256,0,stream>>>(b.X, b.OHb);
+  k_leff<<<dim3(100,512),256,0,stream>>>(b.OHb, k7,b7,k5,b5,k3,b3, b.Qb);
+  k_tbwd<<<dim3(704,16),256,0,stream>>>(b.Qb, b.X);
 
   nystrom_layer(b, l2_lnw, l2_lnb, wqkvT2, woutT2, l2_bout, l2_resk, stream);
   k_copy<<<2,256,0,stream>>>(h2row, b.X, 512);
 
   nystrom_layer(b, l2_lnw, l2_lnb, wqkvT2, woutT2, l2_bout, l2_resk, stream);
 
-  k_ln<<<N1,256,0,stream>>>(b.X, b.Y, l2_lnw, l2_lnb);
-  k_gemm<3><<<dim3(176,1),256,0,stream>>>(b.Y, wqkvT2, nullptr, Q0, K0,
-      nullptr, nullptr, nullptr, nullptr, DIM);
-  k_landmark<<<MM,64,0,stream>>>(Q0, b.QL);
-  k_landmark<<<MM,64,0,stream>>>(K0, b.KL);
-  k_nt64<<<dim3(4,4,1),64,0,stream>>>(b.QL, b.KL, b.A2, 0,0,0, MM);
-  k_softmax256<<<MM,256,0,stream>>>(b.A2);
+  k_ln<<<N1,256,0,stream>>>(b.X, b.Yb, l2_lnw, l2_lnb);
+  k_gemm<3><<<dim3(176,1),256,0,stream>>>(nullptr, b.Yb, wqkvT2, nullptr,
+      Q0, K0, nullptr, nullptr, nullptr, DIM);
+  k_landmark<<<MM,64,0,stream>>>(Q0, QL0f);
+  k_landmark<<<MM,64,0,stream>>>(K0, KL0f);
+  k_nt64<<<dim3(4,4,1),64,0,stream>>>(QL0f, KL0f, b.A2, 0,0,0, MM);
+  k_softmax256<<<MM,256,0,stream>>>(b.A2, b.A2b);
   k_rcsum<<<dim3(MM,2),256,0,stream>>>(b.A2, b.sums, MM);
   k_scale<<<1,256,0,stream>>>(b.sums, b.scl, MM);
-  k_z0<<<MM*MM/256,256,0,stream>>>(b.A2, b.Z0, b.Z0t, b.scl);
-  float *Zc, *Zct;
-  run_pinv(b.A2, b, 1, stream, &Zc, &Zct);
-  k_row1<<<1,256,0,stream>>>(Q0, b.KL, row1);
+  k_z0<<<MM*MM/256,256,0,stream>>>(b.A2, b.Z0b, b.Z0tb, b.scl);
+  us *Zc, *Zct;
+  run_pinv(b.A2b, b, 1, stream, &Zc, &Zct);
+  k_row1<<<1,256,0,stream>>>(Q0, KL0f, row1);
   k_rz<<<1,256,0,stream>>>(row1, Zct, rzv);
-  k_nt64<<<dim3(NPAD/64,4,1),64,0,stream>>>(b.QL, K0, b.Y, 0,0,0, NPAD);
-  k_rowstat<<<MM,256,0,stream>>>(b.Y, mxv, sev);
-  k_aout<<<88,256,0,stream>>>(b.Y, rzv, mxv, sev, out);
+  float* L0 = (float*)b.Yb;
+  k_nt64<<<dim3(NPAD/64,4,1),64,0,stream>>>(QL0f, K0, L0, 0,0,0, NPAD);
+  k_rowstat<<<MM,256,0,stream>>>(L0, mxv, sev);
+  k_aout<<<88,256,0,stream>>>(L0, rzv, mxv, sev, out);
   k_final<<<1,256,0,stream>>>(h2row, nw, nbb, w2, b2, out);
 }
```

Measured after the change: 2.640 ms. 3.6% less time.
